# Kernel optimization log

Hardware: AMD Instinct MI355X
Metric: run time of the kernel (lower is better)

Reference implementation:

```python
import jax, jax.numpy as jnp
import numpy as np
import math

Re = 0.15
DX = 1.0
UB = -1.0
NZ, NY, NX = 64, 256, 256
DT = 0.5
ITERATION = 2

def conv3(x, w, stride=1):
    return jax.lax.conv_general_dilated(x, w, (stride, stride, stride), 'VALID', dimension_numbers=('NCDHW', 'OIDHW', 'NCDHW'))

def pad1(x):
    return jnp.pad(x, ((0, 0), (0, 0), (1, 1), (1, 1), (1, 1)))

def bc_u(u):
    p = pad1(u)
    p = p.at[0, 0, :, :, 0].set(UB)
    p = p.at[0, 0, :, :, -1].set(UB)
    p = p.at[0, 0, :, 0, :].set(p[0, 0, :, 1, :])
    p = p.at[0, 0, :, -1, :].set(p[0, 0, :, -2, :])
    p = p.at[0, 0, 0, :, :].set(0.0)
    p = p.at[0, 0, -1, :, :].set(p[0, 0, -2, :, :])
    return p

def bc_v(v):
    # x faces, y faces, z-bottom are zero -> already satisfied by zero padding
    p = pad1(v)
    p = p.at[0, 0, -1, :, :].set(p[0, 0, -2, :, :])
    return p

def bc_w(w):
    # all six faces zero
    return pad1(w)

def bc_p(q):
    p = pad1(q)
    p = p.at[0, 0, :, :, 0].set(p[0, 0, :, :, 1])
    p = p.at[0, 0, :, :, -1].set(0.0)
    p = p.at[0, 0, :, 0, :].set(p[0, 0, :, 1, :])
    p = p.at[0, 0, :, -1, :].set(p[0, 0, :, -2, :])
    p = p.at[0, 0, 0, :, :].set(p[0, 0, 1, :, :])
    p = p.at[0, 0, -1, :, :].set(p[0, 0, -2, :, :])
    return p

def solid_body(u, v, w, sigma, dt):
    s = 1.0 / (1.0 + dt * sigma)
    return u * s, v * s, w * s

def prol(x):
    # nearest-neighbour upsample x2 in z, y, x
    return jnp.repeat(jnp.repeat(jnp.repeat(x, 2, axis=2), 2, axis=3), 2, axis=4)

def all_ads(uu, vv, ww, w1, w2, w3, w4):
    return (conv3(uu, w2), conv3(uu, w3), conv3(uu, w4),
            conv3(vv, w2), conv3(vv, w3), conv3(vv, w4),
            conv3(ww, w2), conv3(ww, w3), conv3(ww, w4),
            conv3(uu, w1), conv3(vv, w1), conv3(ww, w1))

def pg_vector(uu, vv, ww, u, v, w, k1, sigma, dt, w_diff, ads):
    ADx_u, ADy_u, ADz_u, ADx_v, ADy_v, ADz_v, ADx_w, ADy_w, ADz_w, AD2_u, AD2_v, AD2_w = ads
    speed = jnp.abs(u) * DX + jnp.abs(v) * DX + jnp.abs(w) * DX
    c = DX ** -3
    def kd(AD2, ax, ay, az):
        num = 0.1 * DX * jnp.abs((1.0 / 3.0) * c * speed * AD2)
        den = 0.001 + (jnp.abs(ax) * c + jnp.abs(ay) * c + jnp.abs(az) * c) / 3.0
        return num / den
    inv = 1.0 / (1.0 + dt * sigma)
    k_u = jnp.minimum(kd(AD2_u, ADx_u, ADy_u, ADz_u), k1) * inv
    k_v = jnp.minimum(kd(AD2_v, ADx_v, ADy_v, ADz_v), k1) * inv
    k_w = jnp.minimum(kd(AD2_w, ADx_w, ADy_w, ADz_w), k1) * inv
    # boundary_condition_k zeroes every halo face -> plain zero pad
    kuu, kvv, kww = pad1(k_u), pad1(k_v), pad1(k_w)
    k_x = 0.5 * (k_u * AD2_u + conv3(uu * kuu, w_diff) - u * conv3(kuu, w_diff))
    k_y = 0.5 * (k_v * AD2_v + conv3(vv * kvv, w_diff) - v * conv3(kvv, w_diff))
    k_z = 0.5 * (k_w * AD2_w + conv3(ww * kww, w_diff) - w * conv3(kww, w_diff))
    return k_x, k_y, k_z

def f_cycle_mg(uu, vv, ww, p, wA, w2, w3, w4, w_res, iteration, diag, dt, nlevel, ratio_x, ratio_y):
    b = -(conv3(uu, w2) + conv3(vv, w3) + conv3(ww, w4)) / dt
    w = jnp.zeros((1, 1, 2, 2 * ratio_y, 2 * ratio_x), b.dtype)
    r = b
    for _ in range(iteration):
        w = jnp.zeros((1, 1, 2, 2 * ratio_y, 2 * ratio_x), b.dtype)
        r = conv3(bc_p(p), wA) - b
        r_s = [r]
        for _ in range(1, nlevel - 1):
            r = conv3(r, w_res, stride=2)
            r_s.append(r)
        for i in reversed(range(1, nlevel - 1)):
            # boundary_condition_cw zeroes every halo face -> plain zero pad
            w = w - conv3(pad1(w), wA) / diag + r_s[i] / diag
            w = prol(w)
        p = p - w
        p = p - conv3(bc_p(p), wA) / diag + b / diag
    return p, w, r

def forward(values_u, values_v, values_w, values_p, k1, sigma, wA, w1, w2, w3, w4, w_res, dt, iteration):
    nz, ny, nx = values_u.shape[2], values_u.shape[3], values_u.shape[4]
    nlevel = int(math.log2(min(nx, ny, nz))) + 1
    ratio_x, ratio_y = nx // nz, ny // nz
    diag = wA[0, 0, 1, 1, 1]
    u, v, w = solid_body(values_u, values_v, values_w, sigma, dt)
    uu, vv, ww = bc_u(u), bc_v(v), bc_w(w)
    pp = bc_p(values_p)
    Gpx, Gpy, Gpz = conv3(pp, w2) * dt, conv3(pp, w3) * dt, conv3(pp, w4) * dt
    ads = all_ads(uu, vv, ww, w1, w2, w3, w4)
    k_x, k_y, k_z = pg_vector(uu, vv, ww, u, v, w, k1, sigma, dt, w1, ads)
    ADx_u, ADy_u, ADz_u, ADx_v, ADy_v, ADz_v, ADx_w, ADy_w, ADz_w, AD2_u, AD2_v, AD2_w = ads
    # predictor half step
    b_u = u + 0.5 * (Re * AD2_u * dt - u * ADx_u * dt - v * ADy_u * dt - w * ADz_u * dt) + 0.5 * k_x * dt - Gpx
    b_v = v + 0.5 * (Re * AD2_v * dt - u * ADx_v * dt - v * ADy_v * dt - w * ADz_v * dt) + 0.5 * k_y * dt - Gpy
    b_w = w + 0.5 * (Re * AD2_w * dt - u * ADx_w * dt - v * ADy_w * dt - w * ADz_w * dt) + 0.5 * k_z * dt - Gpz
    b_u, b_v, b_w = solid_body(b_u, b_v, b_w, sigma, dt)
    buu, bvv, bww = bc_u(b_u), bc_v(b_v), bc_w(b_w)
    ads = all_ads(buu, bvv, bww, w1, w2, w3, w4)
    k_x, k_y, k_z = pg_vector(buu, bvv, bww, b_u, b_v, b_w, k1, sigma, dt, w1, ads)
    ADx_u, ADy_u, ADz_u, ADx_v, ADy_v, ADz_v, ADx_w, ADy_w, ADz_w, AD2_u, AD2_v, AD2_w = ads
    # corrector full step
    u = u + Re * AD2_u * dt - b_u * ADx_u * dt - b_v * ADy_u * dt - b_w * ADz_u * dt + k_x * dt - Gpx
    v = v + Re * AD2_v * dt - b_u * ADx_v * dt - b_v * ADy_v * dt - b_w * ADz_v * dt + k_y * dt - Gpy
    w = w + Re * AD2_w * dt - b_u * ADx_w * dt - b_v * ADy_w * dt - b_w * ADz_w * dt + k_z * dt - Gpz
    u, v, w = solid_body(u, v, w, sigma, dt)
    uu, vv, ww = bc_u(u), bc_v(v), bc_w(w)
    p, w_mg, r = f_cycle_mg(uu, vv, ww, values_p, wA, w2, w3, w4, w_res, iteration, diag, dt, nlevel, ratio_x, ratio_y)
    # pressure-gradient velocity correction
    pp = bc_p(p)
    u = u - conv3(pp, w2) * dt
    v = v - conv3(pp, w3) * dt
    w = w - conv3(pp, w4) * dt
    u, v, w = solid_body(u, v, w, sigma, dt)
    return u, v, w, p, w_mg, r

def setup_inputs():
    key = jax.random.key(0)
    ks = jax.random.split(key, 4)
    f32 = jnp.float32
    shp = (1, 1, NZ, NY, NX)
    pshp = (1, 1, NZ + 2, NY + 2, NX + 2)
    lap = np.full((3, 3, 3), 1.0 / 26.0, np.float32)
    lap[1, 1, 1] = -1.0
    wA = jnp.asarray(lap.reshape(1, 1, 3, 3, 3))
    w1 = wA / (DX * DX)
    def cdiff(axis):
        k = np.zeros((3, 3, 3), np.float32)
        idx = [1, 1, 1]
        idx[axis] = 0
        k[tuple(idx)] = -0.5
        idx[axis] = 2
        k[tuple(idx)] = 0.5
        return jnp.asarray(k.reshape(1, 1, 3, 3, 3))
    w4, w3, w2 = cdiff(0), cdiff(1), cdiff(2)  # z, y, x advection stencils
    w_res = jnp.full((1, 1, 2, 2, 2), 0.125, f32)
    return dict(
        values_u=0.1 * jax.random.normal(ks[0], shp, f32),
        values_uu=jnp.zeros(pshp, f32),
        values_v=0.1 * jax.random.normal(ks[1], shp, f32),
        values_vv=jnp.zeros(pshp, f32),
        values_w=0.1 * jax.random.normal(ks[2], shp, f32),
        values_ww=jnp.zeros(pshp, f32),
        values_p=0.1 * jax.random.normal(ks[3], shp, f32),
        values_pp=jnp.zeros(pshp, f32),
        b_uu=jnp.zeros(pshp, f32), b_vv=jnp.zeros(pshp, f32), b_ww=jnp.zeros(pshp, f32),
        k1=2.0 * jnp.ones(shp, f32),
        k_uu=jnp.zeros(pshp, f32), k_vv=jnp.zeros(pshp, f32), k_ww=jnp.zeros(pshp, f32),
        sigma=jnp.zeros(shp, f32),
        wA=wA, w1=w1, w2=w2, w3=w3, w4=w4, w_res=w_res,
        dt=DT, iteration=ITERATION,
    )

def reference(values_u, values_uu, values_v, values_vv, values_w, values_ww, values_p, values_pp, b_uu, b_vv, b_ww, k1, k_uu, k_vv, k_ww, sigma, wA, w1, w2, w3, w4, w_res, dt, iteration):
    # padded scratch buffers (values_uu, ..., k_ww) are fully overwritten by the
    # boundary-condition routines, so the functional version rebuilds them via padding
    return forward(values_u, values_v, values_w, values_p, k1, sigma, wA, w1, w2, w3, w4, w_res, dt, iteration)
```

## Files before the change

### kernel.cpp

```cpp
#include <hip/hip_runtime.h>


#define RE_  0.15f
#define UB_  (-1.0f)
#define NZc  64
#define NYc  256
#define NXc  256
#define PZc  (NZc + 2)
#define PYc  (NYc + 2)
#define PXc  (NXc + 2)
#define Ncell  (NZc * NYc * NXc)
#define PNcell (PZc * PYc * PXc)

#define TBX 32
#define TBY 8
#define TZS 16
#define TLX 34
#define TLY 10
#define PL  340

#define NHALO 198920

__device__ __forceinline__ int PIDX(int z, int y, int x) { return (z * PYc + y) * PXc + x; }
__device__ __forceinline__ int IDX (int z, int y, int x) { return (z * NYc + y) * NXc + x; }

struct F1 { float s, c, xm, xp, ym, yp; };
__device__ __forceinline__ F1 rdf1(const float* sl, int ty, int tx) {
  float t[3][3];
#pragma unroll
  for (int dy = 0; dy < 3; ++dy)
#pragma unroll
    for (int dx = 0; dx < 3; ++dx)
      t[dy][dx] = sl[(ty + dy) * TLX + tx + dx];
  F1 f;
  f.s = t[0][0]+t[0][1]+t[0][2]+t[1][0]+t[1][1]+t[1][2]+t[2][0]+t[2][1]+t[2][2];
  f.c = t[1][1]; f.xm = t[1][0]; f.xp = t[1][2]; f.ym = t[0][1]; f.yp = t[2][1];
  return f;
}

struct F2 { float sv, svk, sk, vc, xm, xp, ym, yp, kc; };
__device__ __forceinline__ F2 rdf2(const float* slv, const float* slk, int ty, int tx) {
  float tv[3][3], tk[3][3];
#pragma unroll
  for (int dy = 0; dy < 3; ++dy)
#pragma unroll
    for (int dx = 0; dx < 3; ++dx) {
      tv[dy][dx] = slv[(ty + dy) * TLX + tx + dx];
      tk[dy][dx] = slk[(ty + dy) * TLX + tx + dx];
    }
  F2 f; f.sv = 0.f; f.svk = 0.f; f.sk = 0.f;
#pragma unroll
  for (int dy = 0; dy < 3; ++dy)
#pragma unroll
    for (int dx = 0; dx < 3; ++dx) {
      f.sv += tv[dy][dx]; f.svk += tv[dy][dx] * tk[dy][dx]; f.sk += tk[dy][dx];
    }
  f.vc = tv[1][1]; f.xm = tv[1][0]; f.xp = tv[1][2]; f.ym = tv[0][1]; f.yp = tv[2][1];
  f.kc = tk[1][1];
  return f;
}

struct R2s { float sv, svk, sk, vc; };
struct R1s { float s, c; };

#define SLOAD(G, pz, t0, t1) { \
    t0 = (G)[PIDX((pz), by0 + q0r, bx0 + q0c)]; \
    if (tid < PL - 256) t1 = (G)[PIDX((pz), by0 + q1r, bx0 + q1c)]; }
#define SWRITE(L, slot, t0, t1) { \
    (L)[(slot)][tid] = t0; \
    if (tid < PL - 256) (L)[(slot)][256 + tid] = t1; }


__global__ __launch_bounds__(256) void k_compute_k_t(
    const float* __restrict__ Au, const float* __restrict__ Av, const float* __restrict__ Aw,
    const float* __restrict__ k1, const float* __restrict__ sigma, const float* __restrict__ dtp,
    const float* __restrict__ w1, const float* __restrict__ wx, const float* __restrict__ wy,
    const float* __restrict__ wz,
    float* __restrict__ Ku, float* __restrict__ Kv, float* __restrict__ Kw) {
  __shared__ float Lu[2][PL], Lv[2][PL], Lw[2][PL];
  const int tx = threadIdx.x, ty = threadIdx.y;
  const int tid = ty * TBX + tx;
  const int bx0 = blockIdx.x * TBX, by0 = blockIdx.y * TBY;
  const int z0 = blockIdx.z * TZS;
  const int q0r = tid / TLX, q0c = tid % TLX;
  const int q1r = (256 + tid) / TLX, q1c = (256 + tid) % TLX;
  const int ix = bx0 + tx, iy = by0 + ty;

  float dt = dtp[0];
  float wo = w1[0], wcd = w1[13] - wo;
  float cxm = wx[12], cxp = wx[14], cym = wy[10], cyp = wy[16], czm = wz[4], czp = wz[22];
  const float third = 1.0f / 3.0f;

  float a0, a1, b0, b1, c0, c1;
  SLOAD(Au, z0, a0, a1); SLOAD(Av, z0, b0, b1); SLOAD(Aw, z0, c0, c1);
  SWRITE(Lu, 0, a0, a1); SWRITE(Lv, 0, b0, b1); SWRITE(Lw, 0, c0, c1);
  __syncthreads();
  F1 fu = rdf1(&Lu[0][0], ty, tx), fv = rdf1(&Lv[0][0], ty, tx), fw = rdf1(&Lw[0][0], ty, tx);
  R1s p0u = {fu.s, fu.c}, p0v = {fv.s, fv.c}, p0w = {fw.s, fw.c};
  SLOAD(Au, z0 + 1, a0, a1); SLOAD(Av, z0 + 1, b0, b1); SLOAD(Aw, z0 + 1, c0, c1);
  SWRITE(Lu, 1, a0, a1); SWRITE(Lv, 1, b0, b1); SWRITE(Lw, 1, c0, c1);
  __syncthreads();
  F1 p1u = rdf1(&Lu[1][0], ty, tx), p1v = rdf1(&Lv[1][0], ty, tx), p1w = rdf1(&Lw[1][0], ty, tx);
  SLOAD(Au, z0 + 2, a0, a1); SLOAD(Av, z0 + 2, b0, b1); SLOAD(Aw, z0 + 2, c0, c1);
  SWRITE(Lu, 0, a0, a1); SWRITE(Lv, 0, b0, b1); SWRITE(Lw, 0, c0, c1);
  __syncthreads();

  for (int iz = z0; iz < z0 + TZS; ++iz) {
    int rs = (iz - z0) & 1, wsl = rs ^ 1;
    int pzn = iz + 3;
    bool do_st = (pzn <= z0 + TZS + 1);
    if (do_st) { SLOAD(Au, pzn, a0, a1); SLOAD(Av, pzn, b0, b1); SLOAD(Aw, pzn, c0, c1); }

    int ci = IDX(iz, iy, ix);
    float inv = 1.0f / (1.0f + dt * sigma[ci]);
    float k1v = k1[ci];
    float speed = fabsf(p1u.c) + fabsf(p1v.c) + fabsf(p1w.c);
    int pc = PIDX(iz + 1, iy + 1, ix + 1);

    fu = rdf1(&Lu[rs][0], ty, tx);
    {
      float ad2 = wo * (p0u.s + p1u.s + fu.s) + wcd * p1u.c;
      float ax = cxm * p1u.xm + cxp * p1u.xp;
      float ay = cym * p1u.ym + cyp * p1u.yp;
      float az = czm * p0u.c + czp * fu.c;
      float num = 0.1f * fabsf(third * speed * ad2);
      float den = 0.001f + (fabsf(ax) + fabsf(ay) + fabsf(az)) * third;
      Ku[pc] = fminf(num / den, k1v) * inv;
    }
    p0u.s = p1u.s; p0u.c = p1u.c; p1u = fu;

    fv = rdf1(&Lv[rs][0], ty, tx);
    {
      float ad2 = wo * (p0v.s + p1v.s + fv.s) + wcd * p1v.c;
      float ax = cxm * p1v.xm + cxp * p1v.xp;
      float ay = cym * p1v.ym + cyp * p1v.yp;
      float az = czm * p0v.c + czp * fv.c;
      float num = 0.1f * fabsf(third * speed * ad2);
      float den = 0.001f + (fabsf(ax) + fabsf(ay) + fabsf(az)) * third;
      Kv[pc] = fminf(num / den, k1v) * inv;
    }
    p0v.s = p1v.s; p0v.c = p1v.c; p1v = fv;

    fw = rdf1(&Lw[rs][0], ty, tx);
    {
      float ad2 = wo * (p0w.s + p1w.s + fw.s) + wcd * p1w.c;
      float ax = cxm * p1w.xm + cxp * p1w.xp;
      float ay = cym * p1w.ym + cyp * p1w.yp;
      float az = czm * p0w.c + czp * fw.c;
      float num = 0.1f * fabsf(third * speed * ad2);
      float den = 0.001f + (fabsf(ax) + fabsf(ay) + fabsf(az)) * third;
      Kw[pc] = fminf(num / den, k1v) * inv;
    }
    p0w.s = p1w.s; p0w.c = p1w.c; p1w = fw;

    if (do_st) { SWRITE(Lu, wsl, a0, a1); SWRITE(Lv, wsl, b0, b1); SWRITE(Lw, wsl, c0, c1); }
    __syncthreads();
  }
}

__global__ __launch_bounds__(256) void k_compute_b_t(
    const float* __restrict__ Au, const float* __restrict__ Av, const float* __restrict__ Aw,
    const float* __restrict__ Ku, const float* __restrict__ Kv, const float* __restrict__ Kw,
    const float* __restrict__ gx, const float* __restrict__ gy, const float* __restrict__ gz,
    const float* __restrict__ sigma, const float* __restrict__ dtp,
    const float* __restrict__ w1, const float* __restrict__ wx, const float* __restrict__ wy,
    const float* __restrict__ wz,
    float* __restrict__ Bu, float* __restrict__ Bv, float* __restrict__ Bw) {
  __shared__ float Lu[2][PL], Lv[2][PL], Lw[2][PL], Lku[2][PL], Lkv[2][PL], Lkw[2][PL];
  const int tx = threadIdx.x, ty = threadIdx.y;
  const int tid = ty * TBX + tx;
  const int bx0 = blockIdx.x * TBX, by0 = blockIdx.y * TBY;
  const int z0 = blockIdx.z * TZS;
  const int q0r = tid / TLX, q0c = tid % TLX;
  const int q1r = (256 + tid) / TLX, q1c = (256 + tid) % TLX;
  const int ix = bx0 + tx, iy = by0 + ty;

  float dt = dtp[0];
  float wo = w1[0], wcd = w1[13] - wo;
  float cxm = wx[12], cxp = wx[14], cym = wy[10], cyp = wy[16], czm = wz[4], czp = wz[22];

  float a0, a1, b0, b1, c0, c1, d0, d1, e0, e1, f0, f1;
#define SLOAD6(pz) { SLOAD(Au, pz, a0, a1); SLOAD(Av, pz, b0, b1); SLOAD(Aw, pz, c0, c1); \
                     SLOAD(Ku, pz, d0, d1); SLOAD(Kv, pz, e0, e1); SLOAD(Kw, pz, f0, f1); }
#define SWRITE6(sl) { SWRITE(Lu, sl, a0, a1); SWRITE(Lv, sl, b0, b1); SWRITE(Lw, sl, c0, c1); \
                      SWRITE(Lku, sl, d0, d1); SWRITE(Lkv, sl, e0, e1); SWRITE(Lkw, sl, f0, f1); }
  SLOAD6(z0); SWRITE6(0); __syncthreads();
  F2 fU = rdf2(&Lu[0][0], &Lku[0][0], ty, tx);
  F2 fV = rdf2(&Lv[0][0], &Lkv[0][0], ty, tx);
  F2 fW = rdf2(&Lw[0][0], &Lkw[0][0], ty, tx);
  R2s p0u = {fU.sv, fU.svk, fU.sk, fU.vc};
  R2s p0v = {fV.sv, fV.svk, fV.sk, fV.vc};
  R2s p0w = {fW.sv, fW.svk, fW.sk, fW.vc};
  SLOAD6(z0 + 1); SWRITE6(1); __syncthreads();
  F2 p1u = rdf2(&Lu[1][0], &Lku[1][0], ty, tx);
  F2 p1v = rdf2(&Lv[1][0], &Lkv[1][0], ty, tx);
  F2 p1w = rdf2(&Lw[1][0], &Lkw[1][0], ty, tx);
  SLOAD6(z0 + 2); SWRITE6(0); __syncthreads();

  for (int iz = z0; iz < z0 + TZS; ++iz) {
    int rs = (iz - z0) & 1, wsl = rs ^ 1;
    int pzn = iz + 3;
    bool do_st = (pzn <= z0 + TZS + 1);
    if (do_st) SLOAD6(pzn);

    int ci = IDX(iz, iy, ix);
    float inv = 1.0f / (1.0f + dt * sigma[ci]);
    float gxv = gx[ci], gyv = gy[ci], gzv = gz[ci];
    float uc = p1u.vc, vc = p1v.vc, wc = p1w.vc;
    int pc = PIDX(iz + 1, iy + 1, ix + 1);

    fU = rdf2(&Lu[rs][0], &Lku[rs][0], ty, tx);
    {
      float ad2 = wo * (p0u.sv + p1u.sv + fU.sv) + wcd * uc;
      float suk = wo * (p0u.svk + p1u.svk + fU.svk) + wcd * uc * p1u.kc;
      float sk  = wo * (p0u.sk + p1u.sk + fU.sk) + wcd * p1u.kc;
      float kx = 0.5f * (p1u.kc * ad2 + suk - uc * sk);
      float ax = cxm * p1u.xm + cxp * p1u.xp;
      float ay = cym * p1u.ym + cyp * p1u.yp;
      float az = czm * p0u.vc + czp * fU.vc;
      float bu = uc + 0.5f * dt * (RE_ * ad2 - uc * ax - vc * ay - wc * az) + 0.5f * kx * dt - gxv;
      Bu[pc] = bu * inv;
    }
    p0u.sv = p1u.sv; p0u.svk = p1u.svk; p0u.sk = p1u.sk; p0u.vc = p1u.vc; p1u = fU;

    fV = rdf2(&Lv[rs][0], &Lkv[rs][0], ty, tx);
    {
      float ad2 = wo * (p0v.sv + p1v.sv + fV.sv) + wcd * vc;
      float suk = wo * (p0v.svk + p1v.svk + fV.svk) + wcd * vc * p1v.kc;
      float sk  = wo * (p0v.sk + p1v.sk + fV.sk) + wcd * p1v.kc;
      float kx = 0.5f * (p1v.kc * ad2 + suk - vc * sk);
      float ax = cxm * p1v.xm + cxp * p1v.xp;
      float ay = cym * p1v.ym + cyp * p1v.yp;
      float az = czm * p0v.vc + czp * fV.vc;
      float bv = vc + 0.5f * dt * (RE_ * ad2 - uc * ax - vc * ay - wc * az) + 0.5f * kx * dt - gyv;
      Bv[pc] = bv * inv;
    }
    p0v.sv = p1v.sv; p0v.svk = p1v.svk; p0v.sk = p1v.sk; p0v.vc = p1v.vc; p1v = fV;

    fW = rdf2(&Lw[rs][0], &Lkw[rs][0], ty, tx);
    {
      float ad2 = wo * (p0w.sv + p1w.sv + fW.sv) + wcd * wc;
      float suk = wo * (p0w.svk + p1w.svk + fW.svk) + wcd * wc * p1w.kc;
      float sk  = wo * (p0w.sk + p1w.sk + fW.sk) + wcd * p1w.kc;
      float kx = 0.5f * (p1w.kc * ad2 + suk - wc * sk);
      float ax = cxm * p1w.xm + cxp * p1w.xp;
      float ay = cym * p1w.ym + cyp * p1w.yp;
      float az = czm * p0w.vc + czp * fW.vc;
      float bw = wc + 0.5f * dt * (RE_ * ad2 - uc * ax - vc * ay - wc * az) + 0.5f * kx * dt - gzv;
      Bw[pc] = bw * inv;
    }
    p0w.sv = p1w.sv; p0w.svk = p1w.svk; p0w.sk = p1w.sk; p0w.vc = p1w.vc; p1w = fW;

    if (do_st) SWRITE6(wsl);
    __syncthreads();
  }
}

__global__ __launch_bounds__(256) void k_corrector_t(
    float* __restrict__ Au, float* __restrict__ Av, float* __restrict__ Aw,
    const float* __restrict__ Bu, const float* __restrict__ Bv, const float* __restrict__ Bw,
    const float* __restrict__ Ku, const float* __restrict__ Kv, const float* __restrict__ Kw,
    const float* __restrict__ gx, const float* __restrict__ gy, const float* __restrict__ gz,
    const float* __restrict__ sigma, const float* __restrict__ dtp,
    const float* __restrict__ w1, const float* __restrict__ wx, const float* __restrict__ wy,
    const float* __restrict__ wz) {
  __shared__ float Lu[2][PL], Lv[2][PL], Lw[2][PL], Lku[2][PL], Lkv[2][PL], Lkw[2][PL];
  const int tx = threadIdx.x, ty = threadIdx.y;
  const int tid = ty * TBX + tx;
  const int bx0 = blockIdx.x * TBX, by0 = blockIdx.y * TBY;
  const int z0 = blockIdx.z * TZS;
  const int q0r = tid / TLX, q0c = tid % TLX;
  const int q1r = (256 + tid) / TLX, q1c = (256 + tid) % TLX;
  const int ix = bx0 + tx, iy = by0 + ty;

  float dt = dtp[0];
  float wo = w1[0], wcd = w1[13] - wo;
  float cxm = wx[12], cxp = wx[14], cym = wy[10], cyp = wy[16], czm = wz[4], czp = wz[22];

  float a0, a1, b0, b1, c0, c1, d0, d1, e0, e1, f0, f1;
#define SLOAD6B(pz) { SLOAD(Bu, pz, a0, a1); SLOAD(Bv, pz, b0, b1); SLOAD(Bw, pz, c0, c1); \
                      SLOAD(Ku, pz, d0, d1); SLOAD(Kv, pz, e0, e1); SLOAD(Kw, pz, f0, f1); }
  SLOAD6B(z0); SWRITE6(0); __syncthreads();
  F2 fU = rdf2(&Lu[0][0], &Lku[0][0], ty, tx);
  F2 fV = rdf2(&Lv[0][0], &Lkv[0][0], ty, tx);
  F2 fW = rdf2(&Lw[0][0], &Lkw[0][0], ty, tx);
  R2s p0u = {fU.sv, fU.svk, fU.sk, fU.vc};
  R2s p0v = {fV.sv, fV.svk, fV.sk, fV.vc};
  R2s p0w = {fW.sv, fW.svk, fW.sk, fW.vc};
  SLOAD6B(z0 + 1); SWRITE6(1); __syncthreads();
  F2 p1u = rdf2(&Lu[1][0], &Lku[1][0], ty, tx);
  F2 p1v = rdf2(&Lv[1][0], &Lkv[1][0], ty, tx);
  F2 p1w = rdf2(&Lw[1][0], &Lkw[1][0], ty, tx);
  SLOAD6B(z0 + 2); SWRITE6(0); __syncthreads();

  for (int iz = z0; iz < z0 + TZS; ++iz) {
    int rs = (iz - z0) & 1, wsl = rs ^ 1;
    int pzn = iz + 3;
    bool do_st = (pzn <= z0 + TZS + 1);
    if (do_st) SLOAD6B(pzn);

    int ci = IDX(iz, iy, ix);
    float inv = 1.0f / (1.0f + dt * sigma[ci]);
    float gxv = gx[ci], gyv = gy[ci], gzv = gz[ci];
    int pc = PIDX(iz + 1, iy + 1, ix + 1);
    float auc = Au[pc], avc = Av[pc], awc = Aw[pc];
    float buc = p1u.vc, bvc = p1v.vc, bwc = p1w.vc;

    fU = rdf2(&Lu[rs][0], &Lku[rs][0], ty, tx);
    float un;
    {
      float ad2 = wo * (p0u.sv + p1u.sv + fU.sv) + wcd * buc;
      float suk = wo * (p0u.svk + p1u.svk + fU.svk) + wcd * buc * p1u.kc;
      float sk  = wo * (p0u.sk + p1u.sk + fU.sk) + wcd * p1u.kc;
      float kx = 0.5f * (p1u.kc * ad2 + suk - buc * sk);
      float ax = cxm * p1u.xm + cxp * p1u.xp;
      float ay = cym * p1u.ym + cyp * p1u.yp;
      float az = czm * p0u.vc + czp * fU.vc;
      un = auc + RE_ * ad2 * dt - buc * ax * dt - bvc * ay * dt - bwc * az * dt + kx * dt - gxv;
    }
    p0u.sv = p1u.sv; p0u.svk = p1u.svk; p0u.sk = p1u.sk; p0u.vc = p1u.vc; p1u = fU;

    fV = rdf2(&Lv[rs][0], &Lkv[rs][0], ty, tx);
    float vn;
    {
      float ad2 = wo * (p0v.sv + p1v.sv + fV.sv) + wcd * bvc;
      float suk = wo * (p0v.svk + p1v.svk + fV.svk) + wcd * bvc * p1v.kc;
      float sk  = wo * (p0v.sk + p1v.sk + fV.sk) + wcd * p1v.kc;
      float kx = 0.5f * (p1v.kc * ad2 + suk - bvc * sk);
      float ax = cxm * p1v.xm + cxp * p1v.xp;
      float ay = cym * p1v.ym + cyp * p1v.yp;
      float az = czm * p0v.vc + czp * fV.vc;
      vn = avc + RE_ * ad2 * dt - buc * ax * dt - bvc * ay * dt - bwc * az * dt + kx * dt - gyv;
    }
    p0v.sv = p1v.sv; p0v.svk = p1v.svk; p0v.sk = p1v.sk; p0v.vc = p1v.vc; p1v = fV;

    fW = rdf2(&Lw[rs][0], &Lkw[rs][0], ty, tx);
    float wn;
    {
      float ad2 = wo * (p0w.sv + p1w.sv + fW.sv) + wcd * bwc;
      float suk = wo * (p0w.svk + p1w.svk + fW.svk) + wcd * bwc * p1w.kc;
      float sk  = wo * (p0w.sk + p1w.sk + fW.sk) + wcd * p1w.kc;
      float kx = 0.5f * (p1w.kc * ad2 + suk - bwc * sk);
      float ax = cxm * p1w.xm + cxp * p1w.xp;
      float ay = cym * p1w.ym + cyp * p1w.yp;
      float az = czm * p0w.vc + czp * fW.vc;
      wn = awc + RE_ * ad2 * dt - buc * ax * dt - bvc * ay * dt - bwc * az * dt + kx * dt - gzv;
    }
    p0w.sv = p1w.sv; p0w.svk = p1w.svk; p0w.sk = p1w.sk; p0w.vc = p1w.vc; p1w = fW;

    Au[pc] = un * inv;
    Av[pc] = vn * inv;
    Aw[pc] = wn * inv;

    if (do_st) SWRITE6(wsl);
    __syncthreads();
  }
}

__global__ __launch_bounds__(256) void k_residual_t(
    const float* __restrict__ pp, const float* __restrict__ wA,
    const float* __restrict__ b, float* __restrict__ r0) {
  __shared__ float Lp[2][PL];
  const int tx = threadIdx.x, ty = threadIdx.y;
  const int tid = ty * TBX + tx;
  const int bx0 = blockIdx.x * TBX, by0 = blockIdx.y * TBY;
  const int z0 = blockIdx.z * TZS;
  const int q0r = tid / TLX, q0c = tid % TLX;
  const int q1r = (256 + tid) / TLX, q1c = (256 + tid) % TLX;
  const int ix = bx0 + tx, iy = by0 + ty;
  float wo = wA[0], wcd = wA[13] - wo;

  float a0, a1;
  SLOAD(pp, z0, a0, a1); SWRITE(Lp, 0, a0, a1); __syncthreads();
  F1 f = rdf1(&Lp[0][0], ty, tx);
  R1s p0 = {f.s, f.c};
  SLOAD(pp, z0 + 1, a0, a1); SWRITE(Lp, 1, a0, a1); __syncthreads();
  F1 p1 = rdf1(&Lp[1][0], ty, tx);
  SLOAD(pp, z0 + 2, a0, a1); SWRITE(Lp, 0, a0, a1); __syncthreads();

  for (int iz = z0; iz < z0 + TZS; ++iz) {
    int rs = (iz - z0) & 1, wsl = rs ^ 1;
    int pzn = iz + 3;
    bool do_st = (pzn <= z0 + TZS + 1);
    if (do_st) SLOAD(pp, pzn, a0, a1);
    int ci = IDX(iz, iy, ix);
    f = rdf1(&Lp[rs][0], ty, tx);
    r0[ci] = wo * (p0.s + p1.s + f.s) + wcd * p1.c - b[ci];
    p0.s = p1.s; p0.c = p1.c; p1 = f;
    if (do_st) SWRITE(Lp, wsl, a0, a1);
    __syncthreads();
  }
}

__global__ __launch_bounds__(256) void k_smooth_t(
    const float* __restrict__ pp, const float* __restrict__ wA,
    const float* __restrict__ b, float* __restrict__ p, float* __restrict__ ppOut) {
  __shared__ float Lp[2][PL];
  const int tx = threadIdx.x, ty = threadIdx.y;
  const int tid = ty * TBX + tx;
  const int bx0 = blockIdx.x * TBX, by0 = blockIdx.y * TBY;
  const int z0 = blockIdx.z * TZS;
  const int q0r = tid / TLX, q0c = tid % TLX;
  const int q1r = (256 + tid) / TLX, q1c = (256 + tid) % TLX;
  const int ix = bx0 + tx, iy = by0 + ty;
  float wo = wA[0], wcd = wA[13] - wo;
  float diag = wA[13];

  float a0, a1;
  SLOAD(pp, z0, a0, a1); SWRITE(Lp, 0, a0, a1); __syncthreads();
  F1 f = rdf1(&Lp[0][0], ty, tx);
  R1s p0 = {f.s, f.c};
  SLOAD(pp, z0 + 1, a0, a1); SWRITE(Lp, 1, a0, a1); __syncthreads();
  F1 p1 = rdf1(&Lp[1][0], ty, tx);
  SLOAD(pp, z0 + 2, a0, a1); SWRITE(Lp, 0, a0, a1); __syncthreads();

  for (int iz = z0; iz < z0 + TZS; ++iz) {
    int rs = (iz - z0) & 1, wsl = rs ^ 1;
    int pzn = iz + 3;
    bool do_st = (pzn <= z0 + TZS + 1);
    if (do_st) SLOAD(pp, pzn, a0, a1);
    int ci = IDX(iz, iy, ix);
    f = rdf1(&Lp[rs][0], ty, tx);
    float lap = wo * (p0.s + p1.s + f.s) + wcd * p1.c;
    float v = p1.c - lap / diag + b[ci] / diag;
    p[ci] = v;
    ppOut[PIDX(iz + 1, iy + 1, ix + 1)] = v;
    p0.s = p1.s; p0.c = p1.c; p1 = f;
    if (do_st) SWRITE(Lp, wsl, a0, a1);
    __syncthreads();
  }
}


__global__ void k_scale_interior(const float* __restrict__ u0, const float* __restrict__ v0,
                                 const float* __restrict__ w0, const float* __restrict__ sigma,
                                 const float* __restrict__ dtp,
                                 float* __restrict__ Au, float* __restrict__ Av, float* __restrict__ Aw) {
  int i = blockIdx.x * blockDim.x + threadIdx.x;
  if (i >= Ncell) return;
  int x = i % NXc; int t = i / NXc; int y = t % NYc; int z = t / NYc;
  float s = 1.0f / (1.0f + dtp[0] * sigma[i]);
  int pi = PIDX(z + 1, y + 1, x + 1);
  Au[pi] = u0[i] * s;
  Av[pi] = v0[i] * s;
  Aw[pi] = w0[i] * s;
}

__device__ __forceinline__ void halo_decode(int t, int& z, int& y, int& x) {
  if (t < 2 * PYc * PXc) {
    z = (t >= PYc * PXc) ? PZc - 1 : 0;
    int r = t % (PYc * PXc);
    y = r / PXc; x = r % PXc;
    return;
  }
  t -= 2 * PYc * PXc;
  if (t < 2 * NZc * PXc) {
    z = 1 + t / (2 * PXc);
    int r = t % (2 * PXc);
    y = (r >= PXc) ? PYc - 1 : 0;
    x = r % PXc;
    return;
  }
  t -= 2 * NZc * PXc;
  z = 1 + t / (2 * NYc);
  int r = t % (2 * NYc);
  x = (r >= NYc) ? PXc - 1 : 0;
  y = 1 + (r % NYc);
}

__global__ void k_halo_uvw(float* __restrict__ Au, float* __restrict__ Av, float* __restrict__ Aw) {
  int t = blockIdx.x * blockDim.x + threadIdx.x;
  if (t >= NHALO) return;
  int z, y, x;
  halo_decode(t, z, y, x);
  int i = PIDX(z, y, x);
  float vu;
  if (z == 0) {
    vu = 0.0f;
  } else {
    int zz = (z == PZc - 1) ? NZc : z;
    if (x == 0 || x == PXc - 1) {
      vu = UB_;
    } else {
      int yy = y < 1 ? 1 : (y > NYc ? NYc : y);
      vu = Au[PIDX(zz, yy, x)];
    }
  }
  Au[i] = vu;
  float vv;
  if (z == 0 || x == 0 || x == PXc - 1 || y == 0 || y == PYc - 1) {
    vv = 0.0f;
  } else {
    vv = Av[PIDX(NZc, y, x)];
  }
  Av[i] = vv;
  Aw[i] = 0.0f;
}

__global__ void k_halo_p(float* __restrict__ pp) {
  int t = blockIdx.x * blockDim.x + threadIdx.x;
  if (t >= NHALO) return;
  int z, y, x;
  halo_decode(t, z, y, x);
  float v;
  if (x == PXc - 1) {
    v = 0.0f;
  } else {
    int zz = z < 1 ? 1 : (z > NZc ? NZc : z);
    int yy = y < 1 ? 1 : (y > NYc ? NYc : y);
    int xx = (x == 0) ? 1 : x;
    v = pp[PIDX(zz, yy, xx)];
  }
  pp[PIDX(z, y, x)] = v;
}

__global__ void k_zero_halo3(float* __restrict__ a, float* __restrict__ b, float* __restrict__ c) {
  int t = blockIdx.x * blockDim.x + threadIdx.x;
  if (t >= NHALO) return;
  int z, y, x;
  halo_decode(t, z, y, x);
  int i = PIDX(z, y, x);
  a[i] = 0.f; b[i] = 0.f; c[i] = 0.f;
}

__global__ void k_pad_p_interior(const float* __restrict__ p, float* __restrict__ pp) {
  int i = blockIdx.x * blockDim.x + threadIdx.x;
  if (i >= Ncell) return;
  int x = i % NXc; int t = i / NXc; int y = t % NYc; int z = t / NYc;
  pp[PIDX(z + 1, y + 1, x + 1)] = p[i];
}

__global__ void k_grad_p(const float* __restrict__ pp, const float* __restrict__ wx,
                         const float* __restrict__ wy, const float* __restrict__ wz,
                         const float* __restrict__ dtp,
                         float* __restrict__ gx, float* __restrict__ gy, float* __restrict__ gz) {
  int i = blockIdx.x * blockDim.x + threadIdx.x;
  if (i >= Ncell) return;
  int x = i % NXc; int t = i / NXc; int y = t % NYc; int z = t / NYc;
  float dt = dtp[0];
  gx[i] = (wx[12] * pp[PIDX(z + 1, y + 1, x)] + wx[14] * pp[PIDX(z + 1, y + 1, x + 2)]) * dt;
  gy[i] = (wy[10] * pp[PIDX(z + 1, y, x + 1)] + wy[16] * pp[PIDX(z + 1, y + 2, x + 1)]) * dt;
  gz[i] = (wz[4] * pp[PIDX(z, y + 1, x + 1)] + wz[22] * pp[PIDX(z + 2, y + 1, x + 1)]) * dt;
}

__global__ void k_div(const float* __restrict__ Au, const float* __restrict__ Av,
                      const float* __restrict__ Aw, const float* __restrict__ wx,
                      const float* __restrict__ wy, const float* __restrict__ wz,
                      const float* __restrict__ dtp, float* __restrict__ b) {
  int i = blockIdx.x * blockDim.x + threadIdx.x;
  if (i >= Ncell) return;
  int x = i % NXc; int t = i / NXc; int y = t % NYc; int z = t / NYc;
  float dx = wx[12] * Au[PIDX(z + 1, y + 1, x)] + wx[14] * Au[PIDX(z + 1, y + 1, x + 2)];
  float dy = wy[10] * Av[PIDX(z + 1, y, x + 1)] + wy[16] * Av[PIDX(z + 1, y + 2, x + 1)];
  float dz = wz[4] * Aw[PIDX(z, y + 1, x + 1)] + wz[22] * Aw[PIDX(z + 2, y + 1, x + 1)];
  b[i] = -(dx + dy + dz) / dtp[0];
}

__global__ void k_copy(const float* __restrict__ s, float* __restrict__ d, int n) {
  int i = blockIdx.x * blockDim.x + threadIdx.x;
  if (i < n) d[i] = s[i];
}

__global__ void k_restrict(const float* __restrict__ in, float* __restrict__ out,
                           int onz, int ony, int onx, const float* __restrict__ wres) {
  int i = blockIdx.x * blockDim.x + threadIdx.x;
  int tot = onz * ony * onx;
  if (i >= tot) return;
  int X = i % onx; int t = i / onx; int Y = t % ony; int Z = t / ony;
  int iny = ony * 2, inx = onx * 2;
  float s = 0.f;
#pragma unroll
  for (int dz = 0; dz < 2; ++dz)
#pragma unroll
    for (int dy = 0; dy < 2; ++dy)
#pragma unroll
      for (int dx = 0; dx < 2; ++dx)
        s += wres[(dz * 2 + dy) * 2 + dx] * in[((2 * Z + dz) * iny + 2 * Y + dy) * inx + 2 * X + dx];
  out[i] = s;
}

__global__ void k_up(const float* __restrict__ win, const float* __restrict__ r,
                     float* __restrict__ wout, int nz, int ny, int nx,
                     const float* __restrict__ wA, int first) {
  int i = blockIdx.x * blockDim.x + threadIdx.x;
  int tot = nz * ny * nx;
  if (i >= tot) return;
  int X = i % nx; int t = i / nx; int Y = t % ny; int Z = t / ny;
  float diag = wA[13];
  float val;
  if (first) {
    val = r[i] / diag;
  } else {
    float lap = 0.f;
#pragma unroll
    for (int dz = 0; dz < 3; ++dz)
#pragma unroll
      for (int dy = 0; dy < 3; ++dy)
#pragma unroll
        for (int dx = 0; dx < 3; ++dx) {
          int zz = Z + dz - 1, yy = Y + dy - 1, xx = X + dx - 1;
          if (zz >= 0 && zz < nz && yy >= 0 && yy < ny && xx >= 0 && xx < nx)
            lap += wA[(dz * 3 + dy) * 3 + dx] * win[(zz * ny + yy) * nx + xx];
        }
    val = win[i] - lap / diag + r[i] / diag;
  }
  int ony = 2 * ny, onx = 2 * nx;
#pragma unroll
  for (int dz = 0; dz < 2; ++dz)
#pragma unroll
    for (int dy = 0; dy < 2; ++dy)
#pragma unroll
      for (int dx = 0; dx < 2; ++dx)
        wout[((2 * Z + dz) * ony + (2 * Y + dy)) * onx + (2 * X + dx)] = val;
}

__global__ void k_sub_f(float* __restrict__ p, const float* __restrict__ w0,
                        float* __restrict__ pp) {
  int i = blockIdx.x * blockDim.x + threadIdx.x;
  if (i >= Ncell) return;
  int x = i % NXc; int t = i / NXc; int y = t % NYc; int z = t / NYc;
  float v = p[i] - w0[i];
  p[i] = v;
  pp[PIDX(z + 1, y + 1, x + 1)] = v;
}

__global__ void k_final(const float* __restrict__ Au, const float* __restrict__ Av,
                        const float* __restrict__ Aw, const float* __restrict__ pp,
                        const float* __restrict__ wx, const float* __restrict__ wy,
                        const float* __restrict__ wz, const float* __restrict__ sigma,
                        const float* __restrict__ dtp,
                        float* __restrict__ ou, float* __restrict__ ov, float* __restrict__ ow) {
  int i = blockIdx.x * blockDim.x + threadIdx.x;
  if (i >= Ncell) return;
  int x = i % NXc; int t = i / NXc; int y = t % NYc; int z = t / NYc;
  float dt = dtp[0];
  float inv = 1.0f / (1.0f + dt * sigma[i]);
  int pc = PIDX(z + 1, y + 1, x + 1);
  float dx = wx[12] * pp[PIDX(z + 1, y + 1, x)] + wx[14] * pp[PIDX(z + 1, y + 1, x + 2)];
  float dy = wy[10] * pp[PIDX(z + 1, y, x + 1)] + wy[16] * pp[PIDX(z + 1, y + 2, x + 1)];
  float dz = wz[4] * pp[PIDX(z, y + 1, x + 1)] + wz[22] * pp[PIDX(z + 2, y + 1, x + 1)];
  ou[i] = (Au[pc] - dx * dt) * inv;
  ov[i] = (Av[pc] - dy * dt) * inv;
  ow[i] = (Aw[pc] - dz * dt) * inv;
}


extern "C" void kernel_launch(void* const* d_in, const int* in_sizes, int n_in,
                              void* d_out, int out_size, void* d_ws, size_t ws_size,
                              hipStream_t stream) {
  (void)in_sizes; (void)n_in; (void)out_size; (void)ws_size;

  const float* values_u = (const float*)d_in[0];
  const float* values_v = (const float*)d_in[2];
  const float* values_w = (const float*)d_in[4];
  const float* values_p = (const float*)d_in[6];
  const float* k1       = (const float*)d_in[11];
  const float* sigma    = (const float*)d_in[15];
  const float* wA       = (const float*)d_in[16];
  const float* w1       = (const float*)d_in[17];
  const float* w2       = (const float*)d_in[18];
  const float* w3       = (const float*)d_in[19];
  const float* w4       = (const float*)d_in[20];
  const float* wres     = (const float*)d_in[21];
  const float* dtp      = (const float*)d_in[22];
  const int ITER = 2;

  float* ws = (float*)d_ws;
  float* Au = ws + 0ll * PNcell;
  float* Av = ws + 1ll * PNcell;
  float* Aw = ws + 2ll * PNcell;
  float* Ku = ws + 3ll * PNcell;
  float* Kv = ws + 4ll * PNcell;
  float* Kw = ws + 5ll * PNcell;
  float* Bu = ws + 6ll * PNcell;
  float* Bv = ws + 7ll * PNcell;
  float* Bw = ws + 8ll * PNcell;
  float* ppA = ws + 9ll * PNcell;
  float* ppB = Ku;
  float* b_rhs = Bu;
  float* r0    = Bv;
  float* r1  = Bw;
  float* r2  = r1 + 524288;
  float* r3  = r2 + 65536;
  float* r4  = r3 + 8192;
  float* w1b = r4 + 1024;
  float* w2b = w1b + 524288;
  float* w3b = w2b + 65536;
  float* w4b = w3b + 8192;

  float* out_u   = (float*)d_out;
  float* out_v   = out_u + Ncell;
  float* out_w   = out_v + Ncell;
  float* out_p   = out_w + Ncell;
  float* out_wmg = out_p + Ncell;
  float* out_r   = out_wmg + Ncell;
  float* gx = out_u; float* gy = out_v; float* gz = out_w;

  const int B = 256;
  const int gN = (Ncell + B - 1) / B;
  const int gH = (NHALO + B - 1) / B;
  dim3 tblk(TBX, TBY, 1);
  dim3 tgrd(NXc / TBX, NYc / TBY, NZc / TZS);

  k_scale_interior<<<gN, B, 0, stream>>>(values_u, values_v, values_w, sigma, dtp, Au, Av, Aw);
  k_halo_uvw<<<gH, B, 0, stream>>>(Au, Av, Aw);
  k_pad_p_interior<<<gN, B, 0, stream>>>(values_p, ppA);
  k_halo_p<<<gH, B, 0, stream>>>(ppA);
  k_grad_p<<<gN, B, 0, stream>>>(ppA, w2, w3, w4, dtp, gx, gy, gz);

  k_zero_halo3<<<gH, B, 0, stream>>>(Ku, Kv, Kw);
  k_compute_k_t<<<tgrd, tblk, 0, stream>>>(Au, Av, Aw, k1, sigma, dtp, w1, w2, w3, w4, Ku, Kv, Kw);
  k_compute_b_t<<<tgrd, tblk, 0, stream>>>(Au, Av, Aw, Ku, Kv, Kw, gx, gy, gz, sigma, dtp,
                                           w1, w2, w3, w4, Bu, Bv, Bw);
  k_halo_uvw<<<gH, B, 0, stream>>>(Bu, Bv, Bw);

  k_compute_k_t<<<tgrd, tblk, 0, stream>>>(Bu, Bv, Bw, k1, sigma, dtp, w1, w2, w3, w4, Ku, Kv, Kw);
  k_corrector_t<<<tgrd, tblk, 0, stream>>>(Au, Av, Aw, Bu, Bv, Bw, Ku, Kv, Kw, gx, gy, gz,
                                           sigma, dtp, w1, w2, w3, w4);
  k_halo_uvw<<<gH, B, 0, stream>>>(Au, Av, Aw);

  k_div<<<gN, B, 0, stream>>>(Au, Av, Aw, w2, w3, w4, dtp, b_rhs);
  k_copy<<<gN, B, 0, stream>>>(values_p, out_p, Ncell);
  for (int it = 0; it < ITER; ++it) {
    k_residual_t<<<tgrd, tblk, 0, stream>>>(ppA, wA, b_rhs, r0);
    k_restrict<<<(524288 + B - 1) / B, B, 0, stream>>>(r0, r1, 32, 128, 128, wres);
    k_restrict<<<(65536 + B - 1) / B, B, 0, stream>>>(r1, r2, 16, 64, 64, wres);
    k_restrict<<<(8192 + B - 1) / B, B, 0, stream>>>(r2, r3, 8, 32, 32, wres);
    k_restrict<<<(1024 + B - 1) / B, B, 0, stream>>>(r3, r4, 4, 16, 16, wres);
    k_restrict<<<1, 128, 0, stream>>>(r4, out_r, 2, 8, 8, wres);
    k_up<<<1, 128, 0, stream>>>(nullptr, out_r, w4b, 2, 8, 8, wA, 1);
    k_up<<<(1024 + B - 1) / B, B, 0, stream>>>(w4b, r4, w3b, 4, 16, 16, wA, 0);
    k_up<<<(8192 + B - 1) / B, B, 0, stream>>>(w3b, r3, w2b, 8, 32, 32, wA, 0);
    k_up<<<(65536 + B - 1) / B, B, 0, stream>>>(w2b, r2, w1b, 16, 64, 64, wA, 0);
    k_up<<<(524288 + B - 1) / B, B, 0, stream>>>(w1b, r1, out_wmg, 32, 128, 128, wA, 0);
    k_sub_f<<<gN, B, 0, stream>>>(out_p, out_wmg, ppB);
    k_halo_p<<<gH, B, 0, stream>>>(ppB);
    k_smooth_t<<<tgrd, tblk, 0, stream>>>(ppB, wA, b_rhs, out_p, ppA);
    k_halo_p<<<gH, B, 0, stream>>>(ppA);
  }

  k_final<<<gN, B, 0, stream>>>(Au, Av, Aw, ppA, w2, w3, w4, sigma, dtp, out_u, out_v, out_w);
}
```

Before: 806.9 us.

## Deepen z-slice prefetch in tiled stencils and fuse elementwise kernels

The tiled stencil kernels now unroll the z loop by two and keep two register staging buffers, so each global load is issued two slices ahead and has more time to overlap with compute. Several elementwise kernels are merged: div with copy, and the last upsample with the subtract-and-pad step. Elementwise kernels also switch to four strided elements per thread. This removes some launches and full-grid passes in exchange for more register pressure and more complex loop code.

```diff
diff --git a/kernel.cpp b/kernel.cpp
--- a/kernel.cpp
+++ b/kernel.cpp
@@ -11,6 +11,7 @@
 #define PXc  (NXc + 2)
 #define Ncell  (NZc * NYc * NXc)
 #define PNcell (PZc * PYc * PXc)
+#define NQ (Ncell / 4)
 
 #define TBX 32
 #define TBY 8
@@ -63,12 +64,47 @@
 struct R2s { float sv, svk, sk, vc; };
 struct R1s { float s, c; };
 
-#define SLOAD(G, pz, t0, t1) { \
-    t0 = (G)[PIDX((pz), by0 + q0r, bx0 + q0c)]; \
-    if (tid < PL - 256) t1 = (G)[PIDX((pz), by0 + q1r, bx0 + q1c)]; }
-#define SWRITE(L, slot, t0, t1) { \
-    (L)[(slot)][tid] = t0; \
-    if (tid < PL - 256) (L)[(slot)][256 + tid] = t1; }
+struct T1 { float a0, a1; };
+struct T3 { float a0, a1, b0, b1, c0, c1; };
+struct T6 { float a0, a1, b0, b1, c0, c1, d0, d1, e0, e1, f0, f1; };
+
+#define LD1M(T, G, pz) { \
+    (T).a0 = (G)[PIDX((pz), by0 + q0r, bx0 + q0c)]; \
+    if (tid < PL - 256) (T).a1 = (G)[PIDX((pz), by0 + q1r, bx0 + q1c)]; }
+#define ST1M(T, L, slot) { \
+    L[(slot)][tid] = (T).a0; \
+    if (tid < PL - 256) L[(slot)][256 + tid] = (T).a1; }
+#define LD3M(T, GA, GB, GC, pz) { \
+    int o0 = PIDX((pz), by0 + q0r, bx0 + q0c); \
+    (T).a0 = (GA)[o0]; (T).b0 = (GB)[o0]; (T).c0 = (GC)[o0]; \
+    if (tid < PL - 256) { int o1 = PIDX((pz), by0 + q1r, bx0 + q1c); \
+      (T).a1 = (GA)[o1]; (T).b1 = (GB)[o1]; (T).c1 = (GC)[o1]; } }
+#define ST3M(T, slot) { \
+    Lu[(slot)][tid] = (T).a0; Lv[(slot)][tid] = (T).b0; Lw[(slot)][tid] = (T).c0; \
+    if (tid < PL - 256) { Lu[(slot)][256 + tid] = (T).a1; Lv[(slot)][256 + tid] = (T).b1; \
+      Lw[(slot)][256 + tid] = (T).c1; } }
+#define LD6M(T, GA, GB, GC, GD, GE, GF, pz) { \
+    int o0 = PIDX((pz), by0 + q0r, bx0 + q0c); \
+    (T).a0 = (GA)[o0]; (T).b0 = (GB)[o0]; (T).c0 = (GC)[o0]; \
+    (T).d0 = (GD)[o0]; (T).e0 = (GE)[o0]; (T).f0 = (GF)[o0]; \
+    if (tid < PL - 256) { int o1 = PIDX((pz), by0 + q1r, bx0 + q1c); \
+      (T).a1 = (GA)[o1]; (T).b1 = (GB)[o1]; (T).c1 = (GC)[o1]; \
+      (T).d1 = (GD)[o1]; (T).e1 = (GE)[o1]; (T).f1 = (GF)[o1]; } }
+#define ST6M(T, slot) { \
+    Lu[(slot)][tid] = (T).a0; Lv[(slot)][tid] = (T).b0; Lw[(slot)][tid] = (T).c0; \
+    Lku[(slot)][tid] = (T).d0; Lkv[(slot)][tid] = (T).e0; Lkw[(slot)][tid] = (T).f0; \
+    if (tid < PL - 256) { Lu[(slot)][256 + tid] = (T).a1; Lv[(slot)][256 + tid] = (T).b1; \
+      Lw[(slot)][256 + tid] = (T).c1; Lku[(slot)][256 + tid] = (T).d1; \
+      Lkv[(slot)][256 + tid] = (T).e1; Lkw[(slot)][256 + tid] = (T).f1; } }
+
+#define TILE_PREAMBLE \
+  const int tx = threadIdx.x, ty = threadIdx.y; \
+  const int tid = ty * TBX + tx; \
+  const int bx0 = blockIdx.x * TBX, by0 = blockIdx.y * TBY; \
+  const int z0 = blockIdx.z * TZS; \
+  const int q0r = tid / TLX, q0c = tid % TLX; \
+  const int q1r = (256 + tid) / TLX, q1c = (256 + tid) % TLX; \
+  const int ix = bx0 + tx, iy = by0 + ty;
 
 
 __global__ __launch_bounds__(256) void k_compute_k_t(
@@ -78,46 +114,30 @@
     const float* __restrict__ wz,
     float* __restrict__ Ku, float* __restrict__ Kv, float* __restrict__ Kw) {
   __shared__ float Lu[2][PL], Lv[2][PL], Lw[2][PL];
-  const int tx = threadIdx.x, ty = threadIdx.y;
-  const int tid = ty * TBX + tx;
-  const int bx0 = blockIdx.x * TBX, by0 = blockIdx.y * TBY;
-  const int z0 = blockIdx.z * TZS;
-  const int q0r = tid / TLX, q0c = tid % TLX;
-  const int q1r = (256 + tid) / TLX, q1c = (256 + tid) % TLX;
-  const int ix = bx0 + tx, iy = by0 + ty;
-
+  TILE_PREAMBLE
   float dt = dtp[0];
   float wo = w1[0], wcd = w1[13] - wo;
   float cxm = wx[12], cxp = wx[14], cym = wy[10], cyp = wy[16], czm = wz[4], czp = wz[22];
   const float third = 1.0f / 3.0f;
 
-  float a0, a1, b0, b1, c0, c1;
-  SLOAD(Au, z0, a0, a1); SLOAD(Av, z0, b0, b1); SLOAD(Aw, z0, c0, c1);
-  SWRITE(Lu, 0, a0, a1); SWRITE(Lv, 0, b0, b1); SWRITE(Lw, 0, c0, c1);
-  __syncthreads();
+  T3 t, tA, tB;
+  LD3M(t, Au, Av, Aw, z0); ST3M(t, 0); __syncthreads();
   F1 fu = rdf1(&Lu[0][0], ty, tx), fv = rdf1(&Lv[0][0], ty, tx), fw = rdf1(&Lw[0][0], ty, tx);
   R1s p0u = {fu.s, fu.c}, p0v = {fv.s, fv.c}, p0w = {fw.s, fw.c};
-  SLOAD(Au, z0 + 1, a0, a1); SLOAD(Av, z0 + 1, b0, b1); SLOAD(Aw, z0 + 1, c0, c1);
-  SWRITE(Lu, 1, a0, a1); SWRITE(Lv, 1, b0, b1); SWRITE(Lw, 1, c0, c1);
+  LD3M(t, Au, Av, Aw, z0 + 1); ST3M(t, 1); __syncthreads();
+  F1 p1u = rdf1(&Lu[1][0], ty, tx), p1v = rdf1(&Lv[1][0], ty, tx), p1w = rdf1(&Lw[1][0], ty, tx);
+  LD3M(tA, Au, Av, Aw, z0 + 2); ST3M(tA, 0);
+  LD3M(tB, Au, Av, Aw, z0 + 3);
   __syncthreads();
-  F1 p1u = rdf1(&Lu[1][0], ty, tx), p1v = rdf1(&Lv[1][0], ty, tx), p1w = rdf1(&Lw[1][0], ty, tx);
-  SLOAD(Au, z0 + 2, a0, a1); SLOAD(Av, z0 + 2, b0, b1); SLOAD(Aw, z0 + 2, c0, c1);
-  SWRITE(Lu, 0, a0, a1); SWRITE(Lv, 0, b0, b1); SWRITE(Lw, 0, c0, c1);
-  __syncthreads();
-
-  for (int iz = z0; iz < z0 + TZS; ++iz) {
-    int rs = (iz - z0) & 1, wsl = rs ^ 1;
-    int pzn = iz + 3;
-    bool do_st = (pzn <= z0 + TZS + 1);
-    if (do_st) { SLOAD(Au, pzn, a0, a1); SLOAD(Av, pzn, b0, b1); SLOAD(Aw, pzn, c0, c1); }
-
+
+  auto body = [&](int iz, int slot) {
     int ci = IDX(iz, iy, ix);
     float inv = 1.0f / (1.0f + dt * sigma[ci]);
     float k1v = k1[ci];
     float speed = fabsf(p1u.c) + fabsf(p1v.c) + fabsf(p1w.c);
     int pc = PIDX(iz + 1, iy + 1, ix + 1);
 
-    fu = rdf1(&Lu[rs][0], ty, tx);
+    fu = rdf1(&Lu[slot][0], ty, tx);
     {
       float ad2 = wo * (p0u.s + p1u.s + fu.s) + wcd * p1u.c;
       float ax = cxm * p1u.xm + cxp * p1u.xp;
@@ -129,7 +149,7 @@
     }
     p0u.s = p1u.s; p0u.c = p1u.c; p1u = fu;
 
-    fv = rdf1(&Lv[rs][0], ty, tx);
+    fv = rdf1(&Lv[slot][0], ty, tx);
     {
       float ad2 = wo * (p0v.s + p1v.s + fv.s) + wcd * p1v.c;
       float ax = cxm * p1v.xm + cxp * p1v.xp;
@@ -141,7 +161,7 @@
     }
     p0v.s = p1v.s; p0v.c = p1v.c; p1v = fv;
 
-    fw = rdf1(&Lw[rs][0], ty, tx);
+    fw = rdf1(&Lw[slot][0], ty, tx);
     {
       float ad2 = wo * (p0w.s + p1w.s + fw.s) + wcd * p1w.c;
       float ax = cxm * p1w.xm + cxp * p1w.xp;
@@ -152,8 +172,18 @@
       Kw[pc] = fminf(num / den, k1v) * inv;
     }
     p0w.s = p1w.s; p0w.c = p1w.c; p1w = fw;
-
-    if (do_st) { SWRITE(Lu, wsl, a0, a1); SWRITE(Lv, wsl, b0, b1); SWRITE(Lw, wsl, c0, c1); }
+  };
+
+  for (int iz = z0; iz < z0 + TZS; iz += 2) {
+    bool ldA = (iz + 4 <= z0 + TZS + 1);
+    if (ldA) LD3M(tA, Au, Av, Aw, iz + 4);
+    body(iz, 0);
+    ST3M(tB, 1);
+    __syncthreads();
+    bool ldB = (iz + 5 <= z0 + TZS + 1);
+    if (ldB) LD3M(tB, Au, Av, Aw, iz + 5);
+    body(iz + 1, 1);
+    if (ldA) ST3M(tA, 0);
     __syncthreads();
   }
 }
@@ -167,49 +197,35 @@
     const float* __restrict__ wz,
     float* __restrict__ Bu, float* __restrict__ Bv, float* __restrict__ Bw) {
   __shared__ float Lu[2][PL], Lv[2][PL], Lw[2][PL], Lku[2][PL], Lkv[2][PL], Lkw[2][PL];
-  const int tx = threadIdx.x, ty = threadIdx.y;
-  const int tid = ty * TBX + tx;
-  const int bx0 = blockIdx.x * TBX, by0 = blockIdx.y * TBY;
-  const int z0 = blockIdx.z * TZS;
-  const int q0r = tid / TLX, q0c = tid % TLX;
-  const int q1r = (256 + tid) / TLX, q1c = (256 + tid) % TLX;
-  const int ix = bx0 + tx, iy = by0 + ty;
-
+  TILE_PREAMBLE
   float dt = dtp[0];
   float wo = w1[0], wcd = w1[13] - wo;
   float cxm = wx[12], cxp = wx[14], cym = wy[10], cyp = wy[16], czm = wz[4], czp = wz[22];
 
-  float a0, a1, b0, b1, c0, c1, d0, d1, e0, e1, f0, f1;
-#define SLOAD6(pz) { SLOAD(Au, pz, a0, a1); SLOAD(Av, pz, b0, b1); SLOAD(Aw, pz, c0, c1); \
-                     SLOAD(Ku, pz, d0, d1); SLOAD(Kv, pz, e0, e1); SLOAD(Kw, pz, f0, f1); }
-#define SWRITE6(sl) { SWRITE(Lu, sl, a0, a1); SWRITE(Lv, sl, b0, b1); SWRITE(Lw, sl, c0, c1); \
-                      SWRITE(Lku, sl, d0, d1); SWRITE(Lkv, sl, e0, e1); SWRITE(Lkw, sl, f0, f1); }
-  SLOAD6(z0); SWRITE6(0); __syncthreads();
+  T6 t, tA, tB;
+  LD6M(t, Au, Av, Aw, Ku, Kv, Kw, z0); ST6M(t, 0); __syncthreads();
   F2 fU = rdf2(&Lu[0][0], &Lku[0][0], ty, tx);
   F2 fV = rdf2(&Lv[0][0], &Lkv[0][0], ty, tx);
   F2 fW = rdf2(&Lw[0][0], &Lkw[0][0], ty, tx);
   R2s p0u = {fU.sv, fU.svk, fU.sk, fU.vc};
   R2s p0v = {fV.sv, fV.svk, fV.sk, fV.vc};
   R2s p0w = {fW.sv, fW.svk, fW.sk, fW.vc};
-  SLOAD6(z0 + 1); SWRITE6(1); __syncthreads();
+  LD6M(t, Au, Av, Aw, Ku, Kv, Kw, z0 + 1); ST6M(t, 1); __syncthreads();
   F2 p1u = rdf2(&Lu[1][0], &Lku[1][0], ty, tx);
   F2 p1v = rdf2(&Lv[1][0], &Lkv[1][0], ty, tx);
   F2 p1w = rdf2(&Lw[1][0], &Lkw[1][0], ty, tx);
-  SLOAD6(z0 + 2); SWRITE6(0); __syncthreads();
-
-  for (int iz = z0; iz < z0 + TZS; ++iz) {
-    int rs = (iz - z0) & 1, wsl = rs ^ 1;
-    int pzn = iz + 3;
-    bool do_st = (pzn <= z0 + TZS + 1);
-    if (do_st) SLOAD6(pzn);
-
+  LD6M(tA, Au, Av, Aw, Ku, Kv, Kw, z0 + 2); ST6M(tA, 0);
+  LD6M(tB, Au, Av, Aw, Ku, Kv, Kw, z0 + 3);
+  __syncthreads();
+
+  auto body = [&](int iz, int slot) {
     int ci = IDX(iz, iy, ix);
     float inv = 1.0f / (1.0f + dt * sigma[ci]);
     float gxv = gx[ci], gyv = gy[ci], gzv = gz[ci];
     float uc = p1u.vc, vc = p1v.vc, wc = p1w.vc;
     int pc = PIDX(iz + 1, iy + 1, ix + 1);
 
-    fU = rdf2(&Lu[rs][0], &Lku[rs][0], ty, tx);
+    fU = rdf2(&Lu[slot][0], &Lku[slot][0], ty, tx);
     {
       float ad2 = wo * (p0u.sv + p1u.sv + fU.sv) + wcd * uc;
       float suk = wo * (p0u.svk + p1u.svk + fU.svk) + wcd * uc * p1u.kc;
@@ -223,7 +239,7 @@
     }
     p0u.sv = p1u.sv; p0u.svk = p1u.svk; p0u.sk = p1u.sk; p0u.vc = p1u.vc; p1u = fU;
 
-    fV = rdf2(&Lv[rs][0], &Lkv[rs][0], ty, tx);
+    fV = rdf2(&Lv[slot][0], &Lkv[slot][0], ty, tx);
     {
       float ad2 = wo * (p0v.sv + p1v.sv + fV.sv) + wcd * vc;
       float suk = wo * (p0v.svk + p1v.svk + fV.svk) + wcd * vc * p1v.kc;
@@ -237,7 +253,7 @@
     }
     p0v.sv = p1v.sv; p0v.svk = p1v.svk; p0v.sk = p1v.sk; p0v.vc = p1v.vc; p1v = fV;
 
-    fW = rdf2(&Lw[rs][0], &Lkw[rs][0], ty, tx);
+    fW = rdf2(&Lw[slot][0], &Lkw[slot][0], ty, tx);
     {
       float ad2 = wo * (p0w.sv + p1w.sv + fW.sv) + wcd * wc;
       float suk = wo * (p0w.svk + p1w.svk + fW.svk) + wcd * wc * p1w.kc;
@@ -250,8 +266,18 @@
       Bw[pc] = bw * inv;
     }
     p0w.sv = p1w.sv; p0w.svk = p1w.svk; p0w.sk = p1w.sk; p0w.vc = p1w.vc; p1w = fW;
-
-    if (do_st) SWRITE6(wsl);
+  };
+
+  for (int iz = z0; iz < z0 + TZS; iz += 2) {
+    bool ldA = (iz + 4 <= z0 + TZS + 1);
+    if (ldA) LD6M(tA, Au, Av, Aw, Ku, Kv, Kw, iz + 4);
+    body(iz, 0);
+    ST6M(tB, 1);
+    __syncthreads();
+    bool ldB = (iz + 5 <= z0 + TZS + 1);
+    if (ldB) LD6M(tB, Au, Av, Aw, Ku, Kv, Kw, iz + 5);
+    body(iz + 1, 1);
+    if (ldA) ST6M(tA, 0);
     __syncthreads();
   }
 }
@@ -265,40 +291,28 @@
     const float* __restrict__ w1, const float* __restrict__ wx, const float* __restrict__ wy,
     const float* __restrict__ wz) {
   __shared__ float Lu[2][PL], Lv[2][PL], Lw[2][PL], Lku[2][PL], Lkv[2][PL], Lkw[2][PL];
-  const int tx = threadIdx.x, ty = threadIdx.y;
-  const int tid = ty * TBX + tx;
-  const int bx0 = blockIdx.x * TBX, by0 = blockIdx.y * TBY;
-  const int z0 = blockIdx.z * TZS;
-  const int q0r = tid / TLX, q0c = tid % TLX;
-  const int q1r = (256 + tid) / TLX, q1c = (256 + tid) % TLX;
-  const int ix = bx0 + tx, iy = by0 + ty;
-
+  TILE_PREAMBLE
   float dt = dtp[0];
   float wo = w1[0], wcd = w1[13] - wo;
   float cxm = wx[12], cxp = wx[14], cym = wy[10], cyp = wy[16], czm = wz[4], czp = wz[22];
 
-  float a0, a1, b0, b1, c0, c1, d0, d1, e0, e1, f0, f1;
-#define SLOAD6B(pz) { SLOAD(Bu, pz, a0, a1); SLOAD(Bv, pz, b0, b1); SLOAD(Bw, pz, c0, c1); \
-                      SLOAD(Ku, pz, d0, d1); SLOAD(Kv, pz, e0, e1); SLOAD(Kw, pz, f0, f1); }
-  SLOAD6B(z0); SWRITE6(0); __syncthreads();
+  T6 t, tA, tB;
+  LD6M(t, Bu, Bv, Bw, Ku, Kv, Kw, z0); ST6M(t, 0); __syncthreads();
   F2 fU = rdf2(&Lu[0][0], &Lku[0][0], ty, tx);
   F2 fV = rdf2(&Lv[0][0], &Lkv[0][0], ty, tx);
   F2 fW = rdf2(&Lw[0][0], &Lkw[0][0], ty, tx);
   R2s p0u = {fU.sv, fU.svk, fU.sk, fU.vc};
   R2s p0v = {fV.sv, fV.svk, fV.sk, fV.vc};
   R2s p0w = {fW.sv, fW.svk, fW.sk, fW.vc};
-  SLOAD6B(z0 + 1); SWRITE6(1); __syncthreads();
+  LD6M(t, Bu, Bv, Bw, Ku, Kv, Kw, z0 + 1); ST6M(t, 1); __syncthreads();
   F2 p1u = rdf2(&Lu[1][0], &Lku[1][0], ty, tx);
   F2 p1v = rdf2(&Lv[1][0], &Lkv[1][0], ty, tx);
   F2 p1w = rdf2(&Lw[1][0], &Lkw[1][0], ty, tx);
-  SLOAD6B(z0 + 2); SWRITE6(0); __syncthreads();
-
-  for (int iz = z0; iz < z0 + TZS; ++iz) {
-    int rs = (iz - z0) & 1, wsl = rs ^ 1;
-    int pzn = iz + 3;
-    bool do_st = (pzn <= z0 + TZS + 1);
-    if (do_st) SLOAD6B(pzn);
-
+  LD6M(tA, Bu, Bv, Bw, Ku, Kv, Kw, z0 + 2); ST6M(tA, 0);
+  LD6M(tB, Bu, Bv, Bw, Ku, Kv, Kw, z0 + 3);
+  __syncthreads();
+
+  auto body = [&](int iz, int slot) {
     int ci = IDX(iz, iy, ix);
     float inv = 1.0f / (1.0f + dt * sigma[ci]);
     float gxv = gx[ci], gyv = gy[ci], gzv = gz[ci];
@@ -306,7 +320,7 @@
     float auc = Au[pc], avc = Av[pc], awc = Aw[pc];
     float buc = p1u.vc, bvc = p1v.vc, bwc = p1w.vc;
 
-    fU = rdf2(&Lu[rs][0], &Lku[rs][0], ty, tx);
+    fU = rdf2(&Lu[slot][0], &Lku[slot][0], ty, tx);
     float un;
     {
       float ad2 = wo * (p0u.sv + p1u.sv + fU.sv) + wcd * buc;
@@ -320,7 +334,7 @@
     }
     p0u.sv = p1u.sv; p0u.svk = p1u.svk; p0u.sk = p1u.sk; p0u.vc = p1u.vc; p1u = fU;
 
-    fV = rdf2(&Lv[rs][0], &Lkv[rs][0], ty, tx);
+    fV = rdf2(&Lv[slot][0], &Lkv[slot][0], ty, tx);
     float vn;
     {
       float ad2 = wo * (p0v.sv + p1v.sv + fV.sv) + wcd * bvc;
@@ -334,7 +348,7 @@
     }
     p0v.sv = p1v.sv; p0v.svk = p1v.svk; p0v.sk = p1v.sk; p0v.vc = p1v.vc; p1v = fV;
 
-    fW = rdf2(&Lw[rs][0], &Lkw[rs][0], ty, tx);
+    fW = rdf2(&Lw[slot][0], &Lkw[slot][0], ty, tx);
     float wn;
     {
       float ad2 = wo * (p0w.sv + p1w.sv + fW.sv) + wcd * bwc;
@@ -351,8 +365,18 @@
     Au[pc] = un * inv;
     Av[pc] = vn * inv;
     Aw[pc] = wn * inv;
-
-    if (do_st) SWRITE6(wsl);
+  };
+
+  for (int iz = z0; iz < z0 + TZS; iz += 2) {
+    bool ldA = (iz + 4 <= z0 + TZS + 1);
+    if (ldA) LD6M(tA, Bu, Bv, Bw, Ku, Kv, Kw, iz + 4);
+    body(iz, 0);
+    ST6M(tB, 1);
+    __syncthreads();
+    bool ldB = (iz + 5 <= z0 + TZS + 1);
+    if (ldB) LD6M(tB, Bu, Bv, Bw, Ku, Kv, Kw, iz + 5);
+    body(iz + 1, 1);
+    if (ldA) ST6M(tA, 0);
     __syncthreads();
   }
 }
@@ -361,33 +385,36 @@
     const float* __restrict__ pp, const float* __restrict__ wA,
     const float* __restrict__ b, float* __restrict__ r0) {
   __shared__ float Lp[2][PL];
-  const int tx = threadIdx.x, ty = threadIdx.y;
-  const int tid = ty * TBX + tx;
-  const int bx0 = blockIdx.x * TBX, by0 = blockIdx.y * TBY;
-  const int z0 = blockIdx.z * TZS;
-  const int q0r = tid / TLX, q0c = tid % TLX;
-  const int q1r = (256 + tid) / TLX, q1c = (256 + tid) % TLX;
-  const int ix = bx0 + tx, iy = by0 + ty;
+  TILE_PREAMBLE
   float wo = wA[0], wcd = wA[13] - wo;
 
-  float a0, a1;
-  SLOAD(pp, z0, a0, a1); SWRITE(Lp, 0, a0, a1); __syncthreads();
+  T1 t, tA, tB;
+  LD1M(t, pp, z0); ST1M(t, Lp, 0); __syncthreads();
   F1 f = rdf1(&Lp[0][0], ty, tx);
   R1s p0 = {f.s, f.c};
-  SLOAD(pp, z0 + 1, a0, a1); SWRITE(Lp, 1, a0, a1); __syncthreads();
+  LD1M(t, pp, z0 + 1); ST1M(t, Lp, 1); __syncthreads();
   F1 p1 = rdf1(&Lp[1][0], ty, tx);
-  SLOAD(pp, z0 + 2, a0, a1); SWRITE(Lp, 0, a0, a1); __syncthreads();
-
-  for (int iz = z0; iz < z0 + TZS; ++iz) {
-    int rs = (iz - z0) & 1, wsl = rs ^ 1;
-    int pzn = iz + 3;
-    bool do_st = (pzn <= z0 + TZS + 1);
-    if (do_st) SLOAD(pp, pzn, a0, a1);
+  LD1M(tA, pp, z0 + 2); ST1M(tA, Lp, 0);
+  LD1M(tB, pp, z0 + 3);
+  __syncthreads();
+
+  auto body = [&](int iz, int slot) {
     int ci = IDX(iz, iy, ix);
-    f = rdf1(&Lp[rs][0], ty, tx);
+    f = rdf1(&Lp[slot][0], ty, tx);
     r0[ci] = wo * (p0.s + p1.s + f.s) + wcd * p1.c - b[ci];
     p0.s = p1.s; p0.c = p1.c; p1 = f;
-    if (do_st) SWRITE(Lp, wsl, a0, a1);
+  };
+
+  for (int iz = z0; iz < z0 + TZS; iz += 2) {
+    bool ldA = (iz + 4 <= z0 + TZS + 1);
+    if (ldA) LD1M(tA, pp, iz + 4);
+    body(iz, 0);
+    ST1M(tB, Lp, 1);
+    __syncthreads();
+    bool ldB = (iz + 5 <= z0 + TZS + 1);
+    if (ldB) LD1M(tB, pp, iz + 5);
+    body(iz + 1, 1);
+    if (ldA) ST1M(tA, Lp, 0);
     __syncthreads();
   }
 }
@@ -396,54 +423,138 @@
     const float* __restrict__ pp, const float* __restrict__ wA,
     const float* __restrict__ b, float* __restrict__ p, float* __restrict__ ppOut) {
   __shared__ float Lp[2][PL];
-  const int tx = threadIdx.x, ty = threadIdx.y;
-  const int tid = ty * TBX + tx;
-  const int bx0 = blockIdx.x * TBX, by0 = blockIdx.y * TBY;
-  const int z0 = blockIdx.z * TZS;
-  const int q0r = tid / TLX, q0c = tid % TLX;
-  const int q1r = (256 + tid) / TLX, q1c = (256 + tid) % TLX;
-  const int ix = bx0 + tx, iy = by0 + ty;
+  TILE_PREAMBLE
   float wo = wA[0], wcd = wA[13] - wo;
   float diag = wA[13];
 
-  float a0, a1;
-  SLOAD(pp, z0, a0, a1); SWRITE(Lp, 0, a0, a1); __syncthreads();
+  T1 t, tA, tB;
+  LD1M(t, pp, z0); ST1M(t, Lp, 0); __syncthreads();
   F1 f = rdf1(&Lp[0][0], ty, tx);
   R1s p0 = {f.s, f.c};
-  SLOAD(pp, z0 + 1, a0, a1); SWRITE(Lp, 1, a0, a1); __syncthreads();
+  LD1M(t, pp, z0 + 1); ST1M(t, Lp, 1); __syncthreads();
   F1 p1 = rdf1(&Lp[1][0], ty, tx);
-  SLOAD(pp, z0 + 2, a0, a1); SWRITE(Lp, 0, a0, a1); __syncthreads();
-
-  for (int iz = z0; iz < z0 + TZS; ++iz) {
-    int rs = (iz - z0) & 1, wsl = rs ^ 1;
-    int pzn = iz + 3;
-    bool do_st = (pzn <= z0 + TZS + 1);
-    if (do_st) SLOAD(pp, pzn, a0, a1);
+  LD1M(tA, pp, z0 + 2); ST1M(tA, Lp, 0);
+  LD1M(tB, pp, z0 + 3);
+  __syncthreads();
+
+  auto body = [&](int iz, int slot) {
     int ci = IDX(iz, iy, ix);
-    f = rdf1(&Lp[rs][0], ty, tx);
+    f = rdf1(&Lp[slot][0], ty, tx);
     float lap = wo * (p0.s + p1.s + f.s) + wcd * p1.c;
     float v = p1.c - lap / diag + b[ci] / diag;
     p[ci] = v;
     ppOut[PIDX(iz + 1, iy + 1, ix + 1)] = v;
     p0.s = p1.s; p0.c = p1.c; p1 = f;
-    if (do_st) SWRITE(Lp, wsl, a0, a1);
-    __syncthreads();
-  }
-}
-
-
-__global__ void k_scale_interior(const float* __restrict__ u0, const float* __restrict__ v0,
-                                 const float* __restrict__ w0, const float* __restrict__ sigma,
-                                 const float* __restrict__ dtp,
-                                 float* __restrict__ Au, float* __restrict__ Av, float* __restrict__ Aw) {
-  int i = blockIdx.x * blockDim.x + threadIdx.x;
-  if (i >= Ncell) return;
-  int x = i % NXc; int t = i / NXc; int y = t % NYc; int z = t / NYc;
-  float s = 1.0f / (1.0f + dtp[0] * sigma[i]);
-  int pi = PIDX(z + 1, y + 1, x + 1);
-  Au[pi] = u0[i] * s;
-  Av[pi] = v0[i] * s;
-  Aw[pi] = w0[i] * s;
+  };
+
+  for (int iz = z0; iz < z0 + TZS; iz += 2) {
+    bool ldA = (iz + 4 <= z0 + TZS + 1);
+    if (ldA) LD1M(tA, pp, iz + 4);
+    body(iz, 0);
+    ST1M(tB, Lp, 1);
+    __syncthreads();
+    bool ldB = (iz + 5 <= z0 + TZS + 1);
+    if (ldB) LD1M(tB, pp, iz + 5);
+    body(iz + 1, 1);
+    if (ldA) ST1M(tA, Lp, 0);
+    __syncthreads();
+  }
+}
+
+
+__global__ void k_scale4(const float* __restrict__ u0, const float* __restrict__ v0,
+                         const float* __restrict__ w0, const float* __restrict__ sigma,
+                         const float* __restrict__ dtp,
+                         float* __restrict__ Au, float* __restrict__ Av, float* __restrict__ Aw) {
+  int t0 = blockIdx.x * blockDim.x + threadIdx.x;
+  if (t0 >= NQ) return;
+  float dt = dtp[0];
+#pragma unroll
+  for (int k = 0; k < 4; ++k) {
+    int i = t0 + k * NQ;
+    int x = i % NXc; int t = i / NXc; int y = t % NYc; int z = t / NYc;
+    float s = 1.0f / (1.0f + dt * sigma[i]);
+    int pi = PIDX(z + 1, y + 1, x + 1);
+    Au[pi] = u0[i] * s;
+    Av[pi] = v0[i] * s;
+    Aw[pi] = w0[i] * s;
+  }
+}
+
+__global__ void k_pad_p4(const float* __restrict__ p, float* __restrict__ pp) {
+  int t0 = blockIdx.x * blockDim.x + threadIdx.x;
+  if (t0 >= NQ) return;
+#pragma unroll
+  for (int k = 0; k < 4; ++k) {
+    int i = t0 + k * NQ;
+    int x = i % NXc; int t = i / NXc; int y = t % NYc; int z = t / NYc;
+    pp[PIDX(z + 1, y + 1, x + 1)] = p[i];
+  }
+}
+
+__global__ void k_grad_p4(const float* __restrict__ pp, const float* __restrict__ wx,
+                          const float* __restrict__ wy, const float* __restrict__ wz,
+                          const float* __restrict__ dtp,
+                          float* __restrict__ gx, float* __restrict__ gy, float* __restrict__ gz) {
+  int t0 = blockIdx.x * blockDim.x + threadIdx.x;
+  if (t0 >= NQ) return;
+  float dt = dtp[0];
+  float cxm = wx[12], cxp = wx[14], cym = wy[10], cyp = wy[16], czm = wz[4], czp = wz[22];
+#pragma unroll
+  for (int k = 0; k < 4; ++k) {
+    int i = t0 + k * NQ;
+    int x = i % NXc; int t = i / NXc; int y = t % NYc; int z = t / NYc;
+    gx[i] = (cxm * pp[PIDX(z + 1, y + 1, x)] + cxp * pp[PIDX(z + 1, y + 1, x + 2)]) * dt;
+    gy[i] = (cym * pp[PIDX(z + 1, y, x + 1)] + cyp * pp[PIDX(z + 1, y + 2, x + 1)]) * dt;
+    gz[i] = (czm * pp[PIDX(z, y + 1, x + 1)] + czp * pp[PIDX(z + 2, y + 1, x + 1)]) * dt;
+  }
+}
+
+__global__ void k_divcopy4(const float* __restrict__ Au, const float* __restrict__ Av,
+                           const float* __restrict__ Aw, const float* __restrict__ wx,
+                           const float* __restrict__ wy, const float* __restrict__ wz,
+                           const float* __restrict__ dtp, const float* __restrict__ psrc,
+                           float* __restrict__ b, float* __restrict__ pdst) {
+  int t0 = blockIdx.x * blockDim.x + threadIdx.x;
+  if (t0 >= NQ) return;
+  float rdt = 1.0f / dtp[0];
+  float cxm = wx[12], cxp = wx[14], cym = wy[10], cyp = wy[16], czm = wz[4], czp = wz[22];
+#pragma unroll
+  for (int k = 0; k < 4; ++k) {
+    int i = t0 + k * NQ;
+    int x = i % NXc; int t = i / NXc; int y = t % NYc; int z = t / NYc;
+    float dx = cxm * Au[PIDX(z + 1, y + 1, x)] + cxp * Au[PIDX(z + 1, y + 1, x + 2)];
+    float dy = cym * Av[PIDX(z + 1, y, x + 1)] + cyp * Av[PIDX(z + 1, y + 2, x + 1)];
+    float dz = czm * Aw[PIDX(z, y + 1, x + 1)] + czp * Aw[PIDX(z + 2, y + 1, x + 1)];
+    b[i] = -(dx + dy + dz) * rdt;
+    pdst[i] = psrc[i];
+  }
+}
+
+__global__ void k_final4(const float* __restrict__ Au, const float* __restrict__ Av,
+                         const float* __restrict__ Aw, const float* __restrict__ pp,
+                         const float* __restrict__ wx, const float* __restrict__ wy,
+                         const float* __restrict__ wz, const float* __restrict__ sigma,
+                         const float* __restrict__ dtp,
+                         float* __restrict__ ou, float* __restrict__ ov, float* __restrict__ ow) {
+  int t0 = blockIdx.x * blockDim.x + threadIdx.x;
+  if (t0 >= NQ) return;
+  float dt = dtp[0];
+  float cxm = wx[12], cxp = wx[14], cym = wy[10], cyp = wy[16], czm = wz[4], czp = wz[22];
+#pragma unroll
+  for (int k = 0; k < 4; ++k) {
+    int i = t0 + k * NQ;
+    int x = i % NXc; int t = i / NXc; int y = t % NYc; int z = t / NYc;
+    float inv = 1.0f / (1.0f + dt * sigma[i]);
+    int pc = PIDX(z + 1, y + 1, x + 1);
+    float dx = cxm * pp[PIDX(z + 1, y + 1, x)] + cxp * pp[PIDX(z + 1, y + 1, x + 2)];
+    float dy = cym * pp[PIDX(z + 1, y, x + 1)] + cyp * pp[PIDX(z + 2 + y - y, y + 2, x + 1)];
+    dy = cym * pp[PIDX(z + 1, y, x + 1)] + cyp * pp[PIDX(z + 1, y + 2, x + 1)];
+    float dz = czm * pp[PIDX(z, y + 1, x + 1)] + czp * pp[PIDX(z + 2, y + 1, x + 1)];
+    ou[i] = (Au[pc] - dx * dt) * inv;
+    ov[i] = (Av[pc] - dy * dt) * inv;
+    ow[i] = (Aw[pc] - dz * dt) * inv;
+  }
 }
 
 __device__ __forceinline__ void halo_decode(int t, int& z, int& y, int& x) {
@@ -523,44 +634,6 @@
   a[i] = 0.f; b[i] = 0.f; c[i] = 0.f;
 }
 
-__global__ void k_pad_p_interior(const float* __restrict__ p, float* __restrict__ pp) {
-  int i = blockIdx.x * blockDim.x + threadIdx.x;
-  if (i >= Ncell) return;
-  int x = i % NXc; int t = i / NXc; int y = t % NYc; int z = t / NYc;
-  pp[PIDX(z + 1, y + 1, x + 1)] = p[i];
-}
-
-__global__ void k_grad_p(const float* __restrict__ pp, const float* __restrict__ wx,
-                         const float* __restrict__ wy, const float* __restrict__ wz,
-                         const float* __restrict__ dtp,
-                         float* __restrict__ gx, float* __restrict__ gy, float* __restrict__ gz) {
-  int i = blockIdx.x * blockDim.x + threadIdx.x;
-  if (i >= Ncell) return;
-  int x = i % NXc; int t = i / NXc; int y = t % NYc; int z = t / NYc;
-  float dt = dtp[0];
-  gx[i] = (wx[12] * pp[PIDX(z + 1, y + 1, x)] + wx[14] * pp[PIDX(z + 1, y + 1, x + 2)]) * dt;
-  gy[i] = (wy[10] * pp[PIDX(z + 1, y, x + 1)] + wy[16] * pp[PIDX(z + 1, y + 2, x + 1)]) * dt;
-  gz[i] = (wz[4] * pp[PIDX(z, y + 1, x + 1)] + wz[22] * pp[PIDX(z + 2, y + 1, x + 1)]) * dt;
-}
-
-__global__ void k_div(const float* __restrict__ Au, const float* __restrict__ Av,
-                      const float* __restrict__ Aw, const float* __restrict__ wx,
-                      const float* __restrict__ wy, const float* __restrict__ wz,
-                      const float* __restrict__ dtp, float* __restrict__ b) {
-  int i = blockIdx.x * blockDim.x + threadIdx.x;
-  if (i >= Ncell) return;
-  int x = i % NXc; int t = i / NXc; int y = t % NYc; int z = t / NYc;
-  float dx = wx[12] * Au[PIDX(z + 1, y + 1, x)] + wx[14] * Au[PIDX(z + 1, y + 1, x + 2)];
-  float dy = wy[10] * Av[PIDX(z + 1, y, x + 1)] + wy[16] * Av[PIDX(z + 1, y + 2, x + 1)];
-  float dz = wz[4] * Aw[PIDX(z, y + 1, x + 1)] + wz[22] * Aw[PIDX(z + 2, y + 1, x + 1)];
-  b[i] = -(dx + dy + dz) / dtp[0];
-}
-
-__global__ void k_copy(const float* __restrict__ s, float* __restrict__ d, int n) {
-  int i = blockIdx.x * blockDim.x + threadIdx.x;
-  if (i < n) d[i] = s[i];
-}
-
 __global__ void k_restrict(const float* __restrict__ in, float* __restrict__ out,
                            int onz, int ony, int onx, const float* __restrict__ wres) {
   int i = blockIdx.x * blockDim.x + threadIdx.x;
@@ -614,34 +687,39 @@
         wout[((2 * Z + dz) * ony + (2 * Y + dy)) * onx + (2 * X + dx)] = val;
 }
 
-__global__ void k_sub_f(float* __restrict__ p, const float* __restrict__ w0,
-                        float* __restrict__ pp) {
+__global__ void k_upsub(const float* __restrict__ win, const float* __restrict__ r,
+                        const float* __restrict__ wA, float* __restrict__ wmg,
+                        float* __restrict__ p, float* __restrict__ ppB) {
+  const int nz = 32, ny = 128, nx = 128;
   int i = blockIdx.x * blockDim.x + threadIdx.x;
-  if (i >= Ncell) return;
-  int x = i % NXc; int t = i / NXc; int y = t % NYc; int z = t / NYc;
-  float v = p[i] - w0[i];
-  p[i] = v;
-  pp[PIDX(z + 1, y + 1, x + 1)] = v;
-}
-
-__global__ void k_final(const float* __restrict__ Au, const float* __restrict__ Av,
-                        const float* __restrict__ Aw, const float* __restrict__ pp,
-                        const float* __restrict__ wx, const float* __restrict__ wy,
-                        const float* __restrict__ wz, const float* __restrict__ sigma,
-                        const float* __restrict__ dtp,
-                        float* __restrict__ ou, float* __restrict__ ov, float* __restrict__ ow) {
-  int i = blockIdx.x * blockDim.x + threadIdx.x;
-  if (i >= Ncell) return;
-  int x = i % NXc; int t = i / NXc; int y = t % NYc; int z = t / NYc;
-  float dt = dtp[0];
-  float inv = 1.0f / (1.0f + dt * sigma[i]);
-  int pc = PIDX(z + 1, y + 1, x + 1);
-  float dx = wx[12] * pp[PIDX(z + 1, y + 1, x)] + wx[14] * pp[PIDX(z + 1, y + 1, x + 2)];
-  float dy = wy[10] * pp[PIDX(z + 1, y, x + 1)] + wy[16] * pp[PIDX(z + 1, y + 2, x + 1)];
-  float dz = wz[4] * pp[PIDX(z, y + 1, x + 1)] + wz[22] * pp[PIDX(z + 2, y + 1, x + 1)];
-  ou[i] = (Au[pc] - dx * dt) * inv;
-  ov[i] = (Av[pc] - dy * dt) * inv;
-  ow[i] = (Aw[pc] - dz * dt) * inv;
+  if (i >= nz * ny * nx) return;
+  int X = i % nx; int t = i / nx; int Y = t % ny; int Z = t / ny;
+  float diag = wA[13];
+  float lap = 0.f;
+#pragma unroll
+  for (int dz = 0; dz < 3; ++dz)
+#pragma unroll
+    for (int dy = 0; dy < 3; ++dy)
+#pragma unroll
+      for (int dx = 0; dx < 3; ++dx) {
+        int zz = Z + dz - 1, yy = Y + dy - 1, xx = X + dx - 1;
+        if (zz >= 0 && zz < nz && yy >= 0 && yy < ny && xx >= 0 && xx < nx)
+          lap += wA[(dz * 3 + dy) * 3 + dx] * win[(zz * ny + yy) * nx + xx];
+      }
+  float val = win[i] - lap / diag + r[i] / diag;
+#pragma unroll
+  for (int dz = 0; dz < 2; ++dz)
+#pragma unroll
+    for (int dy = 0; dy < 2; ++dy)
+#pragma unroll
+      for (int dx = 0; dx < 2; ++dx) {
+        int fz = 2 * Z + dz, fy = 2 * Y + dy, fx = 2 * X + dx;
+        int fi = IDX(fz, fy, fx);
+        wmg[fi] = val;
+        float pv = p[fi] - val;
+        p[fi] = pv;
+        ppB[PIDX(fz + 1, fy + 1, fx + 1)] = pv;
+      }
 }
 
 
@@ -697,16 +775,16 @@
   float* gx = out_u; float* gy = out_v; float* gz = out_w;
 
   const int B = 256;
-  const int gN = (Ncell + B - 1) / B;
+  const int gQ = (NQ + B - 1) / B;
   const int gH = (NHALO + B - 1) / B;
   dim3 tblk(TBX, TBY, 1);
   dim3 tgrd(NXc / TBX, NYc / TBY, NZc / TZS);
 
-  k_scale_interior<<<gN, B, 0, stream>>>(values_u, values_v, values_w, sigma, dtp, Au, Av, Aw);
+  k_scale4<<<gQ, B, 0, stream>>>(values_u, values_v, values_w, sigma, dtp, Au, Av, Aw);
   k_halo_uvw<<<gH, B, 0, stream>>>(Au, Av, Aw);
-  k_pad_p_interior<<<gN, B, 0, stream>>>(values_p, ppA);
+  k_pad_p4<<<gQ, B, 0, stream>>>(values_p, ppA);
   k_halo_p<<<gH, B, 0, stream>>>(ppA);
-  k_grad_p<<<gN, B, 0, stream>>>(ppA, w2, w3, w4, dtp, gx, gy, gz);
+  k_grad_p4<<<gQ, B, 0, stream>>>(ppA, w2, w3, w4, dtp, gx, gy, gz);
 
   k_zero_halo3<<<gH, B, 0, stream>>>(Ku, Kv, Kw);
   k_compute_k_t<<<tgrd, tblk, 0, stream>>>(Au, Av, Aw, k1, sigma, dtp, w1, w2, w3, w4, Ku, Kv, Kw);
@@ -719,8 +797,7 @@
                                            sigma, dtp, w1, w2, w3, w4);
   k_halo_uvw<<<gH, B, 0, stream>>>(Au, Av, Aw);
 
-  k_div<<<gN, B, 0, stream>>>(Au, Av, Aw, w2, w3, w4, dtp, b_rhs);
-  k_copy<<<gN, B, 0, stream>>>(values_p, out_p, Ncell);
+  k_divcopy4<<<gQ, B, 0, stream>>>(Au, Av, Aw, w2, w3, w4, dtp, values_p, b_rhs, out_p);
   for (int it = 0; it < ITER; ++it) {
     k_residual_t<<<tgrd, tblk, 0, stream>>>(ppA, wA, b_rhs, r0);
     k_restrict<<<(524288 + B - 1) / B, B, 0, stream>>>(r0, r1, 32, 128, 128, wres);
@@ -732,12 +809,11 @@
     k_up<<<(1024 + B - 1) / B, B, 0, stream>>>(w4b, r4, w3b, 4, 16, 16, wA, 0);
     k_up<<<(8192 + B - 1) / B, B, 0, stream>>>(w3b, r3, w2b, 8, 32, 32, wA, 0);
     k_up<<<(65536 + B - 1) / B, B, 0, stream>>>(w2b, r2, w1b, 16, 64, 64, wA, 0);
-    k_up<<<(524288 + B - 1) / B, B, 0, stream>>>(w1b, r1, out_wmg, 32, 128, 128, wA, 0);
-    k_sub_f<<<gN, B, 0, stream>>>(out_p, out_wmg, ppB);
+    k_upsub<<<(524288 + B - 1) / B, B, 0, stream>>>(w1b, r1, wA, out_wmg, out_p, ppB);
     k_halo_p<<<gH, B, 0, stream>>>(ppB);
     k_smooth_t<<<tgrd, tblk, 0, stream>>>(ppB, wA, b_rhs, out_p, ppA);
     k_halo_p<<<gH, B, 0, stream>>>(ppA);
   }
 
-  k_final<<<gN, B, 0, stream>>>(Au, Av, Aw, ppA, w2, w3, w4, sigma, dtp, out_u, out_v, out_w);
-}
+  k_final4<<<gQ, B, 0, stream>>>(Au, Av, Aw, ppA, w2, w3, w4, sigma, dtp, out_u, out_v, out_w);
+}
```

Result: no change. 792.9 us (-1.7%).
